# Kernel optimization log

Hardware: AMD Instinct MI355X
Metric: run time of the kernel (lower is better)

## Reference

```python
import jax, jax.numpy as jnp
import numpy as np

N = 2048; K = 2048; D = 256; D_RESHAPE = 800
HA = 256; DA = 128; HK = 128; HC = 128; HS = 256
S = max(10, int(0.1 * K))  # n_sample = 204
BN_SCALE = 1.0 / float(np.sqrt(1.0 + 1e-5))  # eval BatchNorm1d with running stats (0,1)

def leaky(x):
    return jax.nn.leaky_relu(x, 0.01)

def conv2d(x, w, b):
    y = jax.lax.conv_general_dilated(x, w, (1, 1), 'VALID', dimension_numbers=('NCHW', 'OIHW', 'NCHW'))
    return y + b[None, :, None, None]

def maxpool2(x):
    return jax.lax.reduce_window(x, -jnp.inf, jax.lax.max, (1, 1, 2, 2), (1, 1, 2, 2), 'VALID')

def data_transform(x, c1w, c1b, c2w, c2b, ew, eb):
    h = maxpool2(leaky(conv2d(x, c1w, c1b)))   # [n,20,12,12]
    h = maxpool2(leaky(conv2d(h, c2w, c2b)))   # [n,50,4,4]
    h = h.reshape(-1, D_RESHAPE)
    return leaky(h @ ew.T + eb)                # [n,D]

def skip_block(X, w1, b1, w2, b2, w3, b3):
    # Conv1d kernel_size=1 == per-position linear over channels
    X1 = leaky(X @ w1.T + b1) * BN_SCALE       # [n,HC]
    X2 = leaky(X @ w2.T + b2) * BN_SCALE       # [n,HC]
    X3 = leaky(X @ w3.T + b3) * BN_SCALE       # [n,d]
    feat = jax.nn.softmax(X1 @ X2.T, axis=0)   # torch Softmax(dim=1) on [1,n,n] -> axis 0
    return feat @ X3 + X

def mask_scores(A, w1, b1, w2, b2, w3, b3, w4, b4):
    X1 = leaky(A @ w1.T + b1)                  # [n,HK]
    X2 = jnp.tanh(A @ w2.T + b2)               # [n,HK]
    M = X1.T @ X2                              # [HK,HK]
    A3 = leaky(M @ w3.T + b3)                  # [HK,K]
    s = A3.T @ w4[0] + b4[0]                   # [K]
    return jax.nn.softmax(s)

def attention(X, few, feb, vw, vb, uw, ub, aww, awb, ew, eb):
    H = leaky(X @ few.T + feb)                 # [n,HA]
    AV = jnp.tanh(H @ vw.T + vb)
    AU = leaky(H @ uw.T + ub)
    a = leaky((AV * AU) @ aww.T + awb)         # [n,1]
    A = jax.nn.softmax(a.T, axis=1)            # [1,n]
    M = leaky((A @ H) @ ew.T + eb)             # [1,d]
    return M, A

def euclid(X, Y):
    d2 = jnp.sum(X * X, 1)[:, None] + jnp.sum(Y * Y, 1)[None, :] - 2.0 * (X @ Y.T)
    return jnp.sqrt(jnp.maximum(d2, 0.0))


def setup_inputs() -> dict:
    key = jax.random.key(0)
    ks = iter(jax.random.split(key, 70))
    def rn(shape, scale=0.05):
        return jax.random.normal(next(ks), shape, dtype=jnp.float32) * scale
    d = {}
    d['B'] = jax.random.normal(next(ks), (N, 1, 28, 28), dtype=jnp.float32)
    d['KB'] = jax.random.normal(next(ks), (K, 1, 28, 28), dtype=jnp.float32)
    d['dt_c1_w'] = rn((20, 1, 5, 5)); d['dt_c1_b'] = rn((20,))
    d['dt_c2_w'] = rn((50, 20, 5, 5)); d['dt_c2_b'] = rn((50,))
    d['dt_emb_w'] = rn((D, D_RESHAPE)); d['dt_emb_b'] = rn((D,))
    for nm, dd in (('sk1', D), ('sk2', D), ('sk3', K)):
        d[nm + '_w1'] = rn((HC, dd)); d[nm + '_b1'] = rn((HC,))
        d[nm + '_w2'] = rn((HC, dd)); d[nm + '_b2'] = rn((HC,))
        d[nm + '_w3'] = rn((dd, dd)); d[nm + '_b3'] = rn((dd,))
    d['mk_w1'] = rn((HK, K)); d['mk_b1'] = rn((HK,))
    d['mk_w2'] = rn((HK, K)); d['mk_b2'] = rn((HK,))
    d['mk_w3'] = rn((K, HK)); d['mk_b3'] = rn((K,))
    d['mk_w4'] = rn((1, HK)); d['mk_b4'] = rn((1,))
    d['fuse_w'] = rn((D, D + S)); d['fuse_b'] = rn((D,))
    for nm, din in (('a1', D), ('a2', 2 * D)):
        d[nm + '_fe_w'] = rn((HA, din)); d[nm + '_fe_b'] = rn((HA,))
        d[nm + '_v_w'] = rn((DA, HA)); d[nm + '_v_b'] = rn((DA,))
        d[nm + '_u_w'] = rn((DA, HA)); d[nm + '_u_b'] = rn((DA,))
        d[nm + '_aw_w'] = rn((1, DA)); d[nm + '_aw_b'] = rn((1,))
        d[nm + '_emb_w'] = rn((din, HA)); d[nm + '_emb_b'] = rn((din,))
    d['semb_w'] = rn((HS, 2 * D)); d['semb_b'] = rn((HS,))
    d['cls_w'] = rn((1, HS)); d['cls_b'] = rn((1,))
    return d


def reference(B, KB, dt_c1_w, dt_c1_b, dt_c2_w, dt_c2_b, dt_emb_w, dt_emb_b,
              sk1_w1, sk1_b1, sk1_w2, sk1_b2, sk1_w3, sk1_b3,
              sk2_w1, sk2_b1, sk2_w2, sk2_b2, sk2_w3, sk2_b3,
              sk3_w1, sk3_b1, sk3_w2, sk3_b2, sk3_w3, sk3_b3,
              mk_w1, mk_b1, mk_w2, mk_b2, mk_w3, mk_b3, mk_w4, mk_b4,
              fuse_w, fuse_b,
              a1_fe_w, a1_fe_b, a1_v_w, a1_v_b, a1_u_w, a1_u_b, a1_aw_w, a1_aw_b, a1_emb_w, a1_emb_b,
              a2_fe_w, a2_fe_b, a2_v_w, a2_v_b, a2_u_w, a2_u_b, a2_aw_w, a2_aw_b, a2_emb_w, a2_emb_b,
              semb_w, semb_b, cls_w, cls_b):
    B_dt = data_transform(B, dt_c1_w, dt_c1_b, dt_c2_w, dt_c2_b, dt_emb_w, dt_emb_b)
    KB_dt = data_transform(KB, dt_c1_w, dt_c1_b, dt_c2_w, dt_c2_b, dt_emb_w, dt_emb_b)
    Xs = skip_block(B_dt, sk1_w1, sk1_b1, sk1_w2, sk1_b2, sk1_w3, sk1_b3)
    Ks = skip_block(KB_dt, sk2_w1, sk2_b1, sk2_w2, sk2_b2, sk2_w3, sk2_b3)
    # torch detaches the affinity (.detach().numpy())
    aff = euclid(jax.lax.stop_gradient(Xs), jax.lax.stop_gradient(Ks))  # [N,K]
    aff_s = skip_block(aff, sk3_w1, sk3_b1, sk3_w2, sk3_b2, sk3_w3, sk3_b3)
    scores = mask_scores(aff_s, mk_w1, mk_b1, mk_w2, mk_b2, mk_w3, mk_b3, mk_w4, mk_b4)
    idx = jnp.argsort(-scores)[:S]                       # top-S knowledge columns
    B_bag = jax.nn.softmax(aff_s[:, idx], axis=1)        # [N,S], torch Softmax(dim=2)
    B_fuse = leaky(jnp.concatenate([B_dt, B_bag], axis=1) @ fuse_w.T + fuse_b)  # [N,D]
    M1, _ = attention(B_fuse, a1_fe_w, a1_fe_b, a1_v_w, a1_v_b, a1_u_w, a1_u_b, a1_aw_w, a1_aw_b, a1_emb_w, a1_emb_b)
    X2 = jnp.concatenate([B_fuse, jnp.tile(M1, (B_fuse.shape[0], 1))], axis=1)  # [N,2D]
    bvec, A = attention(X2, a2_fe_w, a2_fe_b, a2_v_w, a2_v_b, a2_u_w, a2_u_b, a2_aw_w, a2_aw_b, a2_emb_w, a2_emb_b)
    bvec = leaky(bvec @ semb_w.T + semb_b)               # [1,HS]
    Y = jnp.clip(jax.nn.sigmoid(bvec @ cls_w.T + cls_b), 1e-5, 1.0 - 1e-5)
    return (Y, A)
```

## Files before the change

kernel.cpp:

```cpp
#include <hip/hip_runtime.h>
#include <math.h>

#define LEAKY(x) ((x) > 0.f ? (x) : 0.01f * (x))
static constexpr float BN_SCALE = 0.9999950000374997f;

typedef unsigned short ushort_t;
typedef float f32x4 __attribute__((ext_vector_type(4)));
typedef short bf16x8 __attribute__((ext_vector_type(8)));

__device__ __forceinline__ ushort_t f2bfu(float f) {
  union { float f; unsigned u; } v; v.f = f;
  unsigned r = v.u + 0x7fffu + ((v.u >> 16) & 1u);
  return (ushort_t)(r >> 16);
}
__device__ __forceinline__ float bfu2f(ushort_t u) {
  union { unsigned u; float f; } v; v.u = ((unsigned)u) << 16;
  return v.f;
}

__device__ __forceinline__ void gload16(const ushort_t* g, ushort_t* lds) {
  __builtin_amdgcn_global_load_lds(
      (const __attribute__((address_space(1))) void*)g,
      (__attribute__((address_space(3))) void*)lds, 16, 0, 0);
}

__global__ void fill_out(float* out, int n) {
  int i = blockIdx.x * 256 + threadIdx.x;
  if (i < n) out[i] = 0.25f;
}

struct CvtArgs {
  const float* src[20];
  ushort_t* dst[20];
  int len[20];
};
__global__ void to_bf16_multi(CvtArgs a) {
  for (int s = 0; s < 20; ++s) {
    const float* sp = a.src[s];
    ushort_t* dp = a.dst[s];
    int n = a.len[s];
    for (int i = blockIdx.x * 256 + threadIdx.x; i < n; i += gridDim.x * 256)
      dp[i] = f2bfu(sp[i]);
  }
}

struct BiasPk { const float* a[12]; float* out; };
__global__ void bias_pack(BiasPk p) {
  int b = blockIdx.x, t = threadIdx.x;
  p.out[b * 256 + t] = (t < 128) ? p.a[2 * b][t] : p.a[2 * b + 1][t - 128];
}

__global__ void pad_fuse_bf16(const float* __restrict__ w, ushort_t* __restrict__ wp) {
  int idx = blockIdx.x * 256 + threadIdx.x;
  if (idx >= 256 * 512) return;
  int o = idx >> 9, k = idx & 511;
  wp[idx] = (k < 460) ? f2bfu(w[(size_t)o * 460 + k]) : (ushort_t)0;
}

__launch_bounds__(256)
__global__ void conv12_mfma(const float* __restrict__ imgB, const float* __restrict__ imgK,
                            const float* __restrict__ w1, const float* __restrict__ b1,
                            const ushort_t* __restrict__ w2b, const float* __restrict__ b2,
                            ushort_t* __restrict__ out800) {
  __shared__ __align__(16) char smem[39168];
  ushort_t* sh1u = (ushort_t*)smem;
  float* simg = (float*)(smem + 11520);
  float* sw1  = (float*)(smem + 18688);
  float* b1s  = (float*)(smem + 20928);
  ushort_t* As = (ushort_t*)(smem + 11520);
  ushort_t* Bs = (ushort_t*)(smem + 29952);
  float* Cf = (float*)smem;

  int tid = threadIdx.x;
  int bx = blockIdx.x;
  const float* imgb = (bx < 1024) ? imgB + (size_t)bx * 2 * 784
                                  : imgK + (size_t)(bx - 1024) * 2 * 784;

  for (int i = tid; i < 1568; i += 256) {
    int im = (i >= 784) ? 1 : 0;
    int r = i - im * 784;
    int row = r / 28, col = r - row * 28;
    int sc = (col + (row >> 1)) & 31;
    simg[im * 896 + row * 32 + sc] = imgb[i];
  }
  for (int i = tid; i < 500; i += 256) sw1[i] = w1[i];
  if (tid < 20) b1s[tid] = b1[tid];
  __syncthreads();

  for (int o = tid; o < 1152; o += 256) {
    int im = (o >= 576) ? 1 : 0;
    int rem = o - im * 576;
    int cg = rem / 144;
    int pos = rem - cg * 144;
    int py = pos / 12, px = pos - py * 12;
    int y0 = py * 2, x0 = px * 2;
    float p[6][6];
    #pragma unroll
    for (int yy = 0; yy < 6; ++yy) {
      int rr = y0 + yy;
      int rbase = im * 896 + rr * 32;
      int rot = rr >> 1;
      #pragma unroll
      for (int xx = 0; xx < 6; ++xx)
        p[yy][xx] = simg[rbase + ((x0 + xx + rot) & 31)];
    }
    #pragma unroll
    for (int cc = 0; cc < 5; ++cc) {
      int c = cg * 5 + cc;
      const float* wc = &sw1[c * 25];
      float bb = b1s[c];
      float t0 = bb, t1 = bb, t2 = bb, t3 = bb;
      #pragma unroll
      for (int ky = 0; ky < 5; ++ky)
        #pragma unroll
        for (int kx = 0; kx < 5; ++kx) {
          float wv = wc[ky * 5 + kx];
          t0 += p[ky][kx] * wv;
          t1 += p[ky][kx + 1] * wv;
          t2 += p[ky + 1][kx] * wv;
          t3 += p[ky + 1][kx + 1] * wv;
        }
      float mx = fmaxf(fmaxf(t0, t1), fmaxf(t2, t3));
      sh1u[im * 2880 + c * 144 + pos] = f2bfu(LEAKY(mx));
    }
  }

  int wave = tid >> 6, lane = tid & 63;
  int wm = (wave >> 1) * 64, wn = (wave & 1) * 32;
  int mrow = lane & 15, kq = lane >> 4;
  int kl = tid & 63, rbase = tid >> 6;

  f32x4 acc[4][2];
  #pragma unroll
  for (int i = 0; i < 4; ++i)
    #pragma unroll
    for (int j = 0; j < 2; ++j)
      #pragma unroll
      for (int r = 0; r < 4; ++r) acc[i][j][r] = 0.f;

  for (int k0 = 0; k0 < 512; k0 += 64) {
    __syncthreads();
    int k = k0 + kl;
    bool valid = k < 500;
    int ic = k / 25, tap = k - ic * 25;
    int ky = tap / 5, kx = tap - ky * 5;
    int kof = ic * 144 + ky * 12 + kx;
    ushort_t tA[32];
    #pragma unroll
    for (int i = 0; i < 32; ++i) {
      int r = rbase + 4 * i;
      int im = r >> 6, pos = r & 63, oy = pos >> 3, ox = pos & 7;
      tA[i] = valid ? sh1u[im * 2880 + kof + oy * 12 + ox] : (ushort_t)0;
    }
    ushort_t tB[16];
    #pragma unroll
    for (int i = 0; i < 16; ++i) {
      int oc = rbase + 4 * i;
      tB[i] = (valid && oc < 50) ? w2b[(size_t)oc * 500 + k] : (ushort_t)0;
    }
    #pragma unroll
    for (int i = 0; i < 32; ++i) As[(rbase + 4 * i) * 72 + kl] = tA[i];
    #pragma unroll
    for (int i = 0; i < 16; ++i) Bs[(rbase + 4 * i) * 72 + kl] = tB[i];
    __syncthreads();
    #pragma unroll
    for (int ks = 0; ks < 2; ++ks) {
      bf16x8 af[4], bf[2];
      #pragma unroll
      for (int mt = 0; mt < 4; ++mt)
        af[mt] = *(const bf16x8*)&As[(wm + mt * 16 + mrow) * 72 + ks * 32 + kq * 8];
      #pragma unroll
      for (int nt = 0; nt < 2; ++nt)
        bf[nt] = *(const bf16x8*)&Bs[(wn + nt * 16 + mrow) * 72 + ks * 32 + kq * 8];
      #pragma unroll
      for (int mt = 0; mt < 4; ++mt)
        #pragma unroll
        for (int nt = 0; nt < 2; ++nt)
          acc[mt][nt] = __builtin_amdgcn_mfma_f32_16x16x32_bf16(af[mt], bf[nt], acc[mt][nt], 0, 0, 0);
    }
  }
  __syncthreads();
  #pragma unroll
  for (int mt = 0; mt < 4; ++mt)
    #pragma unroll
    for (int nt = 0; nt < 2; ++nt) {
      int n0 = wn + nt * 16 + (lane & 15);
      #pragma unroll
      for (int r = 0; r < 4; ++r)
        Cf[(wm + mt * 16 + kq * 4 + r) * 68 + n0] = acc[mt][nt][r];
    }
  __syncthreads();
  for (int o = tid; o < 1600; o += 256) {
    int im = o / 800, oi = o - im * 800;
    int oc = oi >> 4, p = oi & 15, py = p >> 2, px = p & 3;
    int r0 = im * 64 + py * 16 + px * 2;
    float bb = b2[oc];
    float t0 = LEAKY(Cf[r0 * 68 + oc] + bb);
    float t1 = LEAKY(Cf[(r0 + 1) * 68 + oc] + bb);
    float t2 = LEAKY(Cf[(r0 + 8) * 68 + oc] + bb);
    float t3 = LEAKY(Cf[(r0 + 9) * 68 + oc] + bb);
    out800[(size_t)(bx * 2 + im) * 800 + oi] = f2bfu(fmaxf(fmaxf(t0, t1), fmaxf(t2, t3)));
  }
}

enum { EPI_NONE = 0, EPI_LEAKY = 1, EPI_LEAKY_BN = 2, EPI_TANH = 3, EPI_EUCLID = 4,
       EPI_LEAKY_BN_ROW = 5, EPI_RES = 6 };

#define LROW 40

template <int EPI>
__launch_bounds__(256)
__global__ void gemm_bf16_nt(const ushort_t* __restrict__ A, const ushort_t* __restrict__ B,
                             const float* __restrict__ bias, float* __restrict__ C32,
                             ushort_t* __restrict__ C16, int M, int N, int Kd,
                             const float* __restrict__ e1, const float* __restrict__ e2) {
  __shared__ __align__(16) ushort_t As[128 * 32];
  __shared__ __align__(16) ushort_t Bs[128 * 32];
  int tid = threadIdx.x;
  int bm = blockIdx.y * 128, bn = blockIdx.x * 128;
  int wave = tid >> 6, lane = tid & 63;
  int wm = (wave >> 1) * 64, wn = (wave & 1) * 64;
  int mrow = lane & 15, kq = lane >> 4;
  int l0 = tid, l1 = tid + 256;
  const ushort_t* ga0 = A + (size_t)(bm + (l0 >> 2)) * Kd + (l0 & 3) * 8;
  const ushort_t* ga1 = A + (size_t)(bm + (l1 >> 2)) * Kd + (l1 & 3) * 8;
  const ushort_t* gb0 = B + (size_t)(bn + (l0 >> 2)) * Kd + (l0 & 3) * 8;
  const ushort_t* gb1 = B + (size_t)(bn + (l1 >> 2)) * Kd + (l1 & 3) * 8;

  f32x4 acc[4][4];
  #pragma unroll
  for (int i = 0; i < 4; ++i)
    #pragma unroll
    for (int j = 0; j < 4; ++j)
      #pragma unroll
      for (int r = 0; r < 4; ++r) acc[i][j][r] = 0.f;

  for (int k0 = 0; k0 < Kd; k0 += 32) {
    __syncthreads();
    gload16(ga0 + k0, &As[l0 * 8]);
    gload16(ga1 + k0, &As[l1 * 8]);
    gload16(gb0 + k0, &Bs[l0 * 8]);
    gload16(gb1 + k0, &Bs[l1 * 8]);
    __syncthreads();
    bf16x8 af[4], bf[4];
    #pragma unroll
    for (int mt = 0; mt < 4; ++mt)
      af[mt] = *(const bf16x8*)&As[(wm + mt * 16 + mrow) * 32 + kq * 8];
    #pragma unroll
    for (int nt = 0; nt < 4; ++nt)
      bf[nt] = *(const bf16x8*)&Bs[(wn + nt * 16 + mrow) * 32 + kq * 8];
    #pragma unroll
    for (int mt = 0; mt < 4; ++mt)
      #pragma unroll
      for (int nt = 0; nt < 4; ++nt)
        acc[mt][nt] = __builtin_amdgcn_mfma_f32_16x16x32_bf16(af[mt], bf[nt], acc[mt][nt], 0, 0, 0);
  }
  #pragma unroll
  for (int mt = 0; mt < 4; ++mt)
    #pragma unroll
    for (int nt = 0; nt < 4; ++nt) {
      int n_g = bn + wn + nt * 16 + (lane & 15);
      #pragma unroll
      for (int r = 0; r < 4; ++r) {
        int m_g = bm + wm + mt * 16 + kq * 4 + r;
        float v = acc[mt][nt][r];
        if (EPI == EPI_EUCLID) {
          v = e1[m_g] + e2[n_g] - 2.f * v;
          v = sqrtf(fmaxf(v, 0.f));
        } else if (EPI == EPI_RES) {
          v += bfu2f(((const ushort_t*)e1)[(size_t)m_g * N + n_g]);
        } else {
          if (bias) v += bias[(EPI == EPI_LEAKY_BN_ROW) ? m_g : n_g];
          if (EPI == EPI_LEAKY) v = LEAKY(v);
          else if (EPI == EPI_LEAKY_BN || EPI == EPI_LEAKY_BN_ROW) { v = LEAKY(v); v *= BN_SCALE; }
          else if (EPI == EPI_TANH) v = tanhf(v);
        }
        if (C32) C32[(size_t)m_g * N + n_g] = v;
        if (C16) C16[(size_t)m_g * N + n_g] = f2bfu(v);
      }
    }
}

__launch_bounds__(256)
__global__ void gemm_smat_z(const ushort_t* __restrict__ X12, ushort_t* __restrict__ Smat) {
  int z = blockIdx.z;
  const ushort_t* A = X12 + (size_t)z * 2048 * 256;
  const ushort_t* B = A + 128;
  ushort_t* C = Smat + (size_t)z * 2048 * 2048;
  __shared__ __align__(16) ushort_t As[128 * 32];
  __shared__ __align__(16) ushort_t Bs[128 * 32];
  int tid = threadIdx.x;
  int bm = blockIdx.y * 128, bn = blockIdx.x * 128;
  int wave = tid >> 6, lane = tid & 63;
  int wm = (wave >> 1) * 64, wn = (wave & 1) * 64;
  int mrow = lane & 15, kq = lane >> 4;
  int l0 = tid, l1 = tid + 256;
  const ushort_t* ga0 = A + (size_t)(bm + (l0 >> 2)) * 256 + (l0 & 3) * 8;
  const ushort_t* ga1 = A + (size_t)(bm + (l1 >> 2)) * 256 + (l1 & 3) * 8;
  const ushort_t* gb0 = B + (size_t)(bn + (l0 >> 2)) * 256 + (l0 & 3) * 8;
  const ushort_t* gb1 = B + (size_t)(bn + (l1 >> 2)) * 256 + (l1 & 3) * 8;

  f32x4 acc[4][4];
  #pragma unroll
  for (int i = 0; i < 4; ++i)
    #pragma unroll
    for (int j = 0; j < 4; ++j)
      #pragma unroll
      for (int r = 0; r < 4; ++r) acc[i][j][r] = 0.f;

  for (int k0 = 0; k0 < 128; k0 += 32) {
    __syncthreads();
    gload16(ga0 + k0, &As[l0 * 8]);
    gload16(ga1 + k0, &As[l1 * 8]);
    gload16(gb0 + k0, &Bs[l0 * 8]);
    gload16(gb1 + k0, &Bs[l1 * 8]);
    __syncthreads();
    bf16x8 af[4], bf[4];
    #pragma unroll
    for (int mt = 0; mt < 4; ++mt)
      af[mt] = *(const bf16x8*)&As[(wm + mt * 16 + mrow) * 32 + kq * 8];
    #pragma unroll
    for (int nt = 0; nt < 4; ++nt)
      bf[nt] = *(const bf16x8*)&Bs[(wn + nt * 16 + mrow) * 32 + kq * 8];
    #pragma unroll
    for (int mt = 0; mt < 4; ++mt)
      #pragma unroll
      for (int nt = 0; nt < 4; ++nt)
        acc[mt][nt] = __builtin_amdgcn_mfma_f32_16x16x32_bf16(af[mt], bf[nt], acc[mt][nt], 0, 0, 0);
  }
  #pragma unroll
  for (int mt = 0; mt < 4; ++mt)
    #pragma unroll
    for (int nt = 0; nt < 4; ++nt) {
      int n_g = bn + wn + nt * 16 + (lane & 15);
      #pragma unroll
      for (int r = 0; r < 4; ++r) {
        int m_g = bm + wm + mt * 16 + kq * 4 + r;
        C[(size_t)m_g * 2048 + n_g] = f2bfu(acc[mt][nt][r]);
      }
    }
}

template <int EPI>
__launch_bounds__(256)
__global__ void gemm_bf16_nt64(const ushort_t* __restrict__ A, const ushort_t* __restrict__ B,
                               const float* __restrict__ bias, float* __restrict__ C32,
                               ushort_t* __restrict__ C16, int M, int N, int Kd) {
  __shared__ __align__(16) ushort_t As[64 * 32];
  __shared__ __align__(16) ushort_t Bs[64 * 32];
  int tid = threadIdx.x;
  int bm = blockIdx.y * 64, bn = blockIdx.x * 64;
  int wave = tid >> 6, lane = tid & 63;
  int wm = (wave >> 1) * 32, wn = (wave & 1) * 32;
  int mrow = lane & 15, kq = lane >> 4;
  const ushort_t* ga = A + (size_t)(bm + (tid >> 2)) * Kd + (tid & 3) * 8;
  const ushort_t* gb = B + (size_t)(bn + (tid >> 2)) * Kd + (tid & 3) * 8;

  f32x4 acc[2][2];
  #pragma unroll
  for (int i = 0; i < 2; ++i)
    #pragma unroll
    for (int j = 0; j < 2; ++j)
      #pragma unroll
      for (int r = 0; r < 4; ++r) acc[i][j][r] = 0.f;

  for (int k0 = 0; k0 < Kd; k0 += 32) {
    __syncthreads();
    gload16(ga + k0, &As[tid * 8]);
    gload16(gb + k0, &Bs[tid * 8]);
    __syncthreads();
    bf16x8 af[2], bf[2];
    #pragma unroll
    for (int mt = 0; mt < 2; ++mt)
      af[mt] = *(const bf16x8*)&As[(wm + mt * 16 + mrow) * 32 + kq * 8];
    #pragma unroll
    for (int nt = 0; nt < 2; ++nt)
      bf[nt] = *(const bf16x8*)&Bs[(wn + nt * 16 + mrow) * 32 + kq * 8];
    #pragma unroll
    for (int mt = 0; mt < 2; ++mt)
      #pragma unroll
      for (int nt = 0; nt < 2; ++nt)
        acc[mt][nt] = __builtin_amdgcn_mfma_f32_16x16x32_bf16(af[mt], bf[nt], acc[mt][nt], 0, 0, 0);
  }
  #pragma unroll
  for (int mt = 0; mt < 2; ++mt)
    #pragma unroll
    for (int nt = 0; nt < 2; ++nt) {
      int n_g = bn + wn + nt * 16 + (lane & 15);
      #pragma unroll
      for (int r = 0; r < 4; ++r) {
        int m_g = bm + wm + mt * 16 + kq * 4 + r;
        float v = acc[mt][nt][r];
        if (bias) v += bias[n_g];
        if (EPI == EPI_LEAKY) v = LEAKY(v);
        else if (EPI == EPI_LEAKY_BN) { v = LEAKY(v); v *= BN_SCALE; }
        else if (EPI == EPI_TANH) v = tanhf(v);
        if (C32) C32[(size_t)m_g * N + n_g] = v;
        if (C16) C16[(size_t)m_g * N + n_g] = f2bfu(v);
      }
    }
}

template <int EPI>
__launch_bounds__(256)
__global__ void gemm_nt64_dual(const ushort_t* __restrict__ A, const ushort_t* __restrict__ B1,
                               const ushort_t* __restrict__ B2, const float* __restrict__ bias1,
                               const float* __restrict__ bias2, ushort_t* __restrict__ C16,
                               int M, int N, int Kd, int Msplit) {
  __shared__ __align__(16) ushort_t As[64 * 32];
  __shared__ __align__(16) ushort_t Bs[64 * 32];
  int tid = threadIdx.x;
  int bm = blockIdx.y * 64, bn = blockIdx.x * 64;
  const ushort_t* B = (bm < Msplit) ? B1 : B2;
  const float* bias = (bm < Msplit) ? bias1 : bias2;
  int wave = tid >> 6, lane = tid & 63;
  int wm = (wave >> 1) * 32, wn = (wave & 1) * 32;
  int mrow = lane & 15, kq = lane >> 4;
  const ushort_t* ga = A + (size_t)(bm + (tid >> 2)) * Kd + (tid & 3) * 8;
  const ushort_t* gb = B + (size_t)(bn + (tid >> 2)) * Kd + (tid & 3) * 8;

  f32x4 acc[2][2];
  #pragma unroll
  for (int i = 0; i < 2; ++i)
    #pragma unroll
    for (int j = 0; j < 2; ++j)
      #pragma unroll
      for (int r = 0; r < 4; ++r) acc[i][j][r] = 0.f;

  for (int k0 = 0; k0 < Kd; k0 += 32) {
    __syncthreads();
    gload16(ga + k0, &As[tid * 8]);
    gload16(gb + k0, &Bs[tid * 8]);
    __syncthreads();
    bf16x8 af[2], bf[2];
    #pragma unroll
    for (int mt = 0; mt < 2; ++mt)
      af[mt] = *(const bf16x8*)&As[(wm + mt * 16 + mrow) * 32 + kq * 8];
    #pragma unroll
    for (int nt = 0; nt < 2; ++nt)
      bf[nt] = *(const bf16x8*)&Bs[(wn + nt * 16 + mrow) * 32 + kq * 8];
    #pragma unroll
    for (int mt = 0; mt < 2; ++mt)
      #pragma unroll
      for (int nt = 0; nt < 2; ++nt)
        acc[mt][nt] = __builtin_amdgcn_mfma_f32_16x16x32_bf16(af[mt], bf[nt], acc[mt][nt], 0, 0, 0);
  }
  #pragma unroll
  for (int mt = 0; mt < 2; ++mt)
    #pragma unroll
    for (int nt = 0; nt < 2; ++nt) {
      int n_g = bn + wn + nt * 16 + (lane & 15);
      #pragma unroll
      for (int r = 0; r < 4; ++r) {
        int m_g = bm + wm + mt * 16 + kq * 4 + r;
        float v = acc[mt][nt][r] + bias[n_g];
        if (EPI == EPI_LEAKY) v = LEAKY(v);
        else if (EPI == EPI_LEAKY_BN) { v = LEAKY(v); v *= BN_SCALE; }
        C16[(size_t)m_g * N + n_g] = f2bfu(v);
      }
    }
}

template <int EPI1, int EPI2>
__launch_bounds__(256)
__global__ void gemm_nt64_split(const ushort_t* __restrict__ A, const ushort_t* __restrict__ B,
                                const float* __restrict__ biasPk, float* __restrict__ C32,
                                ushort_t* __restrict__ C16, int M, int N, int Kd, int Nsplit) {
  __shared__ __align__(16) ushort_t As[64 * 32];
  __shared__ __align__(16) ushort_t Bs[64 * 32];
  int tid = threadIdx.x;
  int bm = blockIdx.y * 64, bn = blockIdx.x * 64;
  int wave = tid >> 6, lane = tid & 63;
  int wm = (wave >> 1) * 32, wn = (wave & 1) * 32;
  int mrow = lane & 15, kq = lane >> 4;
  const ushort_t* ga = A + (size_t)(bm + (tid >> 2)) * Kd + (tid & 3) * 8;
  const ushort_t* gb = B + (size_t)(bn + (tid >> 2)) * Kd + (tid & 3) * 8;

  f32x4 acc[2][2];
  #pragma unroll
  for (int i = 0; i < 2; ++i)
    #pragma unroll
    for (int j = 0; j < 2; ++j)
      #pragma unroll
      for (int r = 0; r < 4; ++r) acc[i][j][r] = 0.f;

  for (int k0 = 0; k0 < Kd; k0 += 32) {
    __syncthreads();
    gload16(ga + k0, &As[tid * 8]);
    gload16(gb + k0, &Bs[tid * 8]);
    __syncthreads();
    bf16x8 af[2], bf[2];
    #pragma unroll
    for (int mt = 0; mt < 2; ++mt)
      af[mt] = *(const bf16x8*)&As[(wm + mt * 16 + mrow) * 32 + kq * 8];
    #pragma unroll
    for (int nt = 0; nt < 2; ++nt)
      bf[nt] = *(const bf16x8*)&Bs[(wn + nt * 16 + mrow) * 32 + kq * 8];
    #pragma unroll
    for (int mt = 0; mt < 2; ++mt)
      #pragma unroll
      for (int nt = 0; nt < 2; ++nt)
        acc[mt][nt] = __builtin_amdgcn_mfma_f32_16x16x32_bf16(af[mt], bf[nt], acc[mt][nt], 0, 0, 0);
  }
  #pragma unroll
  for (int mt = 0; mt < 2; ++mt)
    #pragma unroll
    for (int nt = 0; nt < 2; ++nt) {
      int n_g = bn + wn + nt * 16 + (lane & 15);
      #pragma unroll
      for (int r = 0; r < 4; ++r) {
        int m_g = bm + wm + mt * 16 + kq * 4 + r;
        float v = acc[mt][nt][r] + biasPk[n_g];
        if (n_g < Nsplit) {
          if (EPI1 == EPI_LEAKY) v = LEAKY(v);
          else if (EPI1 == EPI_TANH) v = tanhf(v);
        } else {
          if (EPI2 == EPI_LEAKY) v = LEAKY(v);
          else if (EPI2 == EPI_TANH) v = tanhf(v);
        }
        if (C32) C32[(size_t)m_g * N + n_g] = v;
        if (C16) C16[(size_t)m_g * N + n_g] = f2bfu(v);
      }
    }
}

__launch_bounds__(256)
__global__ void gemm_w3T_z(const ushort_t* __restrict__ W3a, const ushort_t* __restrict__ W3b,
                           const float* __restrict__ b3a, const float* __restrict__ b3b,
                           const ushort_t* __restrict__ dtb, ushort_t* __restrict__ X3T) {
  const int N = 2048, Kd = 256;
  int z = blockIdx.z;
  const ushort_t* A = z ? W3b : W3a;
  const float* bias = z ? b3b : b3a;
  const ushort_t* B = dtb + (size_t)z * 2048 * 256;
  ushort_t* C = X3T + (size_t)z * 256 * 2048;
  __shared__ __align__(16) ushort_t As[64 * 32];
  __shared__ __align__(16) ushort_t Bs[64 * 32];
  int tid = threadIdx.x;
  int bm = blockIdx.y * 64, bn = blockIdx.x * 64;
  int wave = tid >> 6, lane = tid & 63;
  int wm = (wave >> 1) * 32, wn = (wave & 1) * 32;
  int mrow = lane & 15, kq = lane >> 4;
  const ushort_t* ga = A + (size_t)(bm + (tid >> 2)) * Kd + (tid & 3) * 8;
  const ushort_t* gb = B + (size_t)(bn + (tid >> 2)) * Kd + (tid & 3) * 8;

  f32x4 acc[2][2];
  #pragma unroll
  for (int i = 0; i < 2; ++i)
    #pragma unroll
    for (int j = 0; j < 2; ++j)
      #pragma unroll
      for (int r = 0; r < 4; ++r) acc[i][j][r] = 0.f;

  for (int k0 = 0; k0 < Kd; k0 += 32) {
    __syncthreads();
    gload16(ga + k0, &As[tid * 8]);
    gload16(gb + k0, &Bs[tid * 8]);
    __syncthreads();
    bf16x8 af[2], bf[2];
    #pragma unroll
    for (int mt = 0; mt < 2; ++mt)
      af[mt] = *(const bf16x8*)&As[(wm + mt * 16 + mrow) * 32 + kq * 8];
    #pragma unroll
    for (int nt = 0; nt < 2; ++nt)
      bf[nt] = *(const bf16x8*)&Bs[(wn + nt * 16 + mrow) * 32 + kq * 8];
    #pragma unroll
    for (int mt = 0; mt < 2; ++mt)
      #pragma unroll
      for (int nt = 0; nt < 2; ++nt)
        acc[mt][nt] = __builtin_amdgcn_mfma_f32_16x16x32_bf16(af[mt], bf[nt], acc[mt][nt], 0, 0, 0);
  }
  #pragma unroll
  for (int mt = 0; mt < 2; ++mt)
    #pragma unroll
    for (int nt = 0; nt < 2; ++nt) {
      int n_g = bn + wn + nt * 16 + (lane & 15);
      #pragma unroll
      for (int r = 0; r < 4; ++r) {
        int m_g = bm + wm + mt * 16 + kq * 4 + r;
        float v = acc[mt][nt][r] + bias[m_g];
        v = LEAKY(v); v *= BN_SCALE;
        C[(size_t)m_g * N + n_g] = f2bfu(v);
      }
    }
}

__launch_bounds__(256)
__global__ void gemm_ntt_res64_z(const ushort_t* __restrict__ SmatBase,
                                 const ushort_t* __restrict__ X3T,
                                 const ushort_t* __restrict__ dtb,
                                 ushort_t* __restrict__ XsKs) {
  const int N = 256, Kd = 2048;
  int z = blockIdx.z;
  const ushort_t* A = SmatBase + (size_t)z * 2048 * 2048;
  const ushort_t* B = X3T + (size_t)z * 256 * 2048;
  const ushort_t* R = dtb + (size_t)z * 2048 * 256;
  ushort_t* C = XsKs + (size_t)z * 2048 * 256;
  __shared__ __align__(16) ushort_t As[64 * 32];
  __shared__ __align__(16) ushort_t Bs[64 * 32];
  int tid = threadIdx.x;
  int bm = blockIdx.y * 64, bn = blockIdx.x * 64;
  int wave = tid >> 6, lane = tid & 63;
  int wm = (wave >> 1) * 32, wn = (wave & 1) * 32;
  int mrow = lane & 15, kq = lane >> 4;
  const ushort_t* ga = A + (size_t)(bm + (tid >> 2)) * Kd + (tid & 3) * 8;
  const ushort_t* gb = B + (size_t)(bn + (tid >> 2)) * Kd + (tid & 3) * 8;

  f32x4 acc[2][2];
  #pragma unroll
  for (int i = 0; i < 2; ++i)
    #pragma unroll
    for (int j = 0; j < 2; ++j)
      #pragma unroll
      for (int r = 0; r < 4; ++r) acc[i][j][r] = 0.f;

  for (int k0 = 0; k0 < Kd; k0 += 32) {
    __syncthreads();
    gload16(ga + k0, &As[tid * 8]);
    gload16(gb + k0, &Bs[tid * 8]);
    __syncthreads();
    bf16x8 af[2], bf[2];
    #pragma unroll
    for (int mt = 0; mt < 2; ++mt)
      af[mt] = *(const bf16x8*)&As[(wm + mt * 16 + mrow) * 32 + kq * 8];
    #pragma unroll
    for (int nt = 0; nt < 2; ++nt)
      bf[nt] = *(const bf16x8*)&Bs[(wn + nt * 16 + mrow) * 32 + kq * 8];
    #pragma unroll
    for (int mt = 0; mt < 2; ++mt)
      #pragma unroll
      for (int nt = 0; nt < 2; ++nt)
        acc[mt][nt] = __builtin_amdgcn_mfma_f32_16x16x32_bf16(af[mt], bf[nt], acc[mt][nt], 0, 0, 0);
  }
  #pragma unroll
  for (int mt = 0; mt < 2; ++mt)
    #pragma unroll
    for (int nt = 0; nt < 2; ++nt) {
      int n_g = bn + wn + nt * 16 + (lane & 15);
      #pragma unroll
      for (int r = 0; r < 4; ++r) {
        int m_g = bm + wm + mt * 16 + kq * 4 + r;
        float v = acc[mt][nt][r] + bfu2f(R[(size_t)m_g * N + n_g]);
        C[(size_t)m_g * N + n_g] = f2bfu(v);
      }
    }
}

__global__ void gemm_tn_part(const ushort_t* __restrict__ X, float* __restrict__ part) {
  int tx = threadIdx.x & 15, ty = threadIdx.x >> 4;
  int i = blockIdx.y * 16 + ty, j = blockIdx.x * 16 + tx;
  int ks = blockIdx.z;
  float acc = 0.f;
  for (int k = ks * 128; k < ks * 128 + 128; ++k)
    acc += bfu2f(X[(size_t)k * 256 + i]) * bfu2f(X[(size_t)k * 256 + 128 + j]);
  part[(size_t)ks * 16384 + i * 128 + j] = acc;
}
__global__ void gemm_tn_reduce(const float* __restrict__ part, ushort_t* __restrict__ Mm) {
  int idx = blockIdx.x * 256 + threadIdx.x;
  float s = 0.f;
  #pragma unroll
  for (int ks = 0; ks < 16; ++ks) s += part[(size_t)ks * 16384 + idx];
  Mm[idx] = f2bfu(s);
}

__global__ void smax_partA(const ushort_t* __restrict__ Sb, float* __restrict__ pm,
                           float* __restrict__ pl, int N) {
  int z = blockIdx.z;
  const ushort_t* S = Sb + (size_t)z * 2048 * 2048;
  int t = threadIdx.x;
  int col = blockIdx.x * 64 + (t & 63);
  int g = t >> 6;
  int r0 = blockIdx.y * 128 + g;
  float vals[32];
  #pragma unroll
  for (int i = 0; i < 32; ++i)
    vals[i] = bfu2f(S[(size_t)(r0 + 4 * i) * N + col]);
  float m = -1e30f;
  #pragma unroll
  for (int i = 0; i < 32; ++i) m = fmaxf(m, vals[i]);
  float l = 0.f;
  #pragma unroll
  for (int i = 0; i < 32; ++i) l += expf(vals[i] - m);
  __shared__ float rm[4][64], rl[4][64];
  rm[g][t & 63] = m; rl[g][t & 63] = l;
  __syncthreads();
  if (g == 0) {
    int c = t & 63;
    float M0 = rm[0][c], L0 = rl[0][c];
    #pragma unroll
    for (int j = 1; j < 4; ++j) {
      float Mj = rm[j][c], Lj = rl[j][c];
      float nm = fmaxf(M0, Mj);
      L0 = L0 * expf(M0 - nm) + Lj * expf(Mj - nm);
      M0 = nm;
    }
    pm[((size_t)z * 16 + blockIdx.y) * N + col] = M0;
    pl[((size_t)z * 16 + blockIdx.y) * N + col] = L0;
  }
}
__global__ void smax_partB(const float* __restrict__ pm, const float* __restrict__ pl,
                           float* __restrict__ gm, float* __restrict__ gi, int N) {
  int z = blockIdx.y;
  int col = blockIdx.x * 256 + threadIdx.x;
  float m = -1e30f, l = 0.f;
  for (int b = 0; b < 16; ++b) {
    float bm = pm[((size_t)z * 16 + b) * N + col], bl = pl[((size_t)z * 16 + b) * N + col];
    float nm = fmaxf(m, bm);
    l = l * expf(m - nm) + bl * expf(bm - nm);
    m = nm;
  }
  gm[(size_t)z * N + col] = m;
  gi[(size_t)z * N + col] = 1.f / l;
}
__global__ void smax_partC(ushort_t* __restrict__ Sb, const float* __restrict__ gm,
                           const float* __restrict__ gi, int N) {
  int z = blockIdx.z;
  ushort_t* S = Sb + (size_t)z * 2048 * 2048;
  int t = threadIdx.x;
  int col = blockIdx.x * 64 + (t & 63);
  int g = t >> 6;
  float m = gm[(size_t)z * N + col], inv = gi[(size_t)z * N + col];
  int r0 = blockIdx.y * 128 + g;
  #pragma unroll 8
  for (int i = 0; i < 32; ++i) {
    size_t idx = (size_t)(r0 + 4 * i) * N + col;
    S[idx] = f2bfu(expf(bfu2f(S[idx]) - m) * inv);
  }
}

__global__ void row_norm_bf16(const ushort_t* __restrict__ X, float* __restrict__ out, int Kd) {
  int r = blockIdx.x;
  int t = threadIdx.x;
  float s = 0.f;
  for (int k = t; k < Kd; k += 64) { float v = bfu2f(X[(size_t)r * Kd + k]); s += v * v; }
  for (int off = 32; off; off >>= 1) s += __shfl_down(s, off);
  if (t == 0) out[r] = s;
}

__global__ void mask_score(const float* __restrict__ A3, const float* __restrict__ w4,
                           const float* __restrict__ b4, float* __restrict__ s) {
  int k = blockIdx.x * 256 + threadIdx.x;
  float acc = b4[0];
  for (int h = 0; h < 128; ++h) acc += A3[(size_t)h * 2048 + k] * w4[h];
  s[k] = acc;
}

__global__ void topk_rank(const float* __restrict__ s, int* __restrict__ idx, int K, int S) {
  __shared__ float sv[2048];
  int t = threadIdx.x;
  for (int i = t; i < K; i += 256) sv[i] = s[i];
  __syncthreads();
  int j = blockIdx.x * 256 + t;
  if (j >= K) return;
  float sj = sv[j];
  int rank = 0;
  #pragma unroll 8
  for (int i = 0; i < 2048; ++i) {
    float si = sv[i];
    rank += (si > sj) || (si == sj && i < j);
  }
  if (rank < S) idx[rank] = j;
}

__global__ void build_cat(const ushort_t* __restrict__ Bdt, const ushort_t* __restrict__ affs,
                          const int* __restrict__ idx, ushort_t* __restrict__ cat) {
  int r = blockIdx.x, t = threadIdx.x;
  __shared__ float vals[256];
  __shared__ float red[256];
  float v = -1e30f;
  if (t < 204) {
    int ix = idx[t];
    ix = ix < 0 ? 0 : (ix > 2047 ? 2047 : ix);
    v = bfu2f(affs[(size_t)r * 2048 + ix]);
  }
  vals[t] = v;
  red[t] = v;
  __syncthreads();
  for (int off = 128; off; off >>= 1) { if (t < off) red[t] = fmaxf(red[t], red[t + off]); __syncthreads(); }
  float m = red[0];
  __syncthreads();
  float e = (t < 204) ? expf(vals[t] - m) : 0.f;
  red[t] = e;
  __syncthreads();
  for (int off = 128; off; off >>= 1) { if (t < off) red[t] += red[t + off]; __syncthreads(); }
  float inv = 1.f / red[0];
  cat[(size_t)r * 512 + t] = Bdt[(size_t)r * 256 + t];
  cat[(size_t)r * 512 + 256 + t] = (t < 204) ? f2bfu(e * inv) : (ushort_t)0;
}

__global__ void attn_gate(const float* __restrict__ AVU, const float* __restrict__ aww,
                          const float* __restrict__ awb, float* __restrict__ a, int n) {
  int wave = threadIdx.x >> 6, lane = threadIdx.x & 63;
  int r = blockIdx.x * 4 + wave;
  if (r >= n) return;
  float s = 0.f;
  #pragma unroll
  for (int j = 0; j < 2; ++j) {
    int d = lane + 64 * j;
    s += AVU[(size_t)r * 256 + d] * AVU[(size_t)r * 256 + 128 + d] * aww[d];
  }
  for (int off = 32; off; off >>= 1) s += __shfl_down(s, off);
  if (lane == 0) {
    float acc = s + awb[0];
    a[r] = LEAKY(acc);
  }
}

__global__ void softmax_vec(const float* __restrict__ x, float* __restrict__ y,
                            float* __restrict__ y2, int n) {
  __shared__ float red[256];
  int t = threadIdx.x;
  float m = -1e30f;
  for (int i = t; i < n; i += 256) m = fmaxf(m, x[i]);
  red[t] = m;
  __syncthreads();
  for (int off = 128; off; off >>= 1) { if (t < off) red[t] = fmaxf(red[t], red[t + off]); __syncthreads(); }
  m = red[0];
  __syncthreads();
  float s = 0.f;
  for (int i = t; i < n; i += 256) s += expf(x[i] - m);
  red[t] = s;
  __syncthreads();
  for (int off = 128; off; off >>= 1) { if (t < off) red[t] += red[t + off]; __syncthreads(); }
  float inv = 1.f / red[0];
  for (int i = t; i < n; i += 256) {
    float v = expf(x[i] - m) * inv;
    y[i] = v;
    if (y2) y2[i] = v;
  }
}

__global__ void colsum_part(const float* __restrict__ wv, const ushort_t* __restrict__ H,
                            float* __restrict__ part, int n) {
  int bk = blockIdx.x, c = threadIdx.x;
  float s = 0.f;
  for (int r = bk; r < n; r += 16) s += wv[r] * bfu2f(H[(size_t)r * 256 + c]);
  part[bk * 256 + c] = s;
}
__global__ void colsum_fin(const float* __restrict__ part, float* __restrict__ out) {
  int c = threadIdx.x;
  float s = 0.f;
  #pragma unroll
  for (int k = 0; k < 16; ++k) s += part[k * 256 + c];
  out[c] = s;
}

__global__ void gemv_act(const float* __restrict__ x, const float* __restrict__ W,
                         const float* __restrict__ b, float* __restrict__ out,
                         int O, int Kd, int act) {
  int o = blockIdx.x * blockDim.x + threadIdx.x;
  if (o >= O) return;
  float acc = b ? b[o] : 0.f;
  for (int k = 0; k < Kd; ++k) acc += x[k] * W[(size_t)o * Kd + k];
  if (act == 1) acc = LEAKY(acc);
  out[o] = acc;
}

__global__ void build_cat2(const ushort_t* __restrict__ Bf, const float* __restrict__ M1,
                           ushort_t* __restrict__ cat2) {
  int r = blockIdx.x, t = threadIdx.x;
  cat2[(size_t)r * 512 + t] = (t < 256) ? Bf[(size_t)r * 256 + t] : f2bfu(M1[t - 256]);
}

__global__ void final_head(const float* __restrict__ AH2, const float* __restrict__ embw,
                           const float* __restrict__ embb, const float* __restrict__ sembw,
                           const float* __restrict__ sembb, const float* __restrict__ clsw,
                           const float* __restrict__ clsb, float* __restrict__ Yout) {
  __shared__ float bvec[512];
  __shared__ float red[512];
  int t = threadIdx.x;
  float acc = embb[t];
  for (int c = 0; c < 256; ++c) acc += AH2[c] * embw[(size_t)t * 256 + c];
  bvec[t] = LEAKY(acc);
  __syncthreads();
  float p = 0.f;
  if (t < 256) {
    float a2 = sembb[t];
    for (int c = 0; c < 512; ++c) a2 += bvec[c] * sembw[(size_t)t * 512 + c];
    a2 = LEAKY(a2);
    p = a2 * clsw[t];
  }
  red[t] = p;
  __syncthreads();
  for (int off = 256; off; off >>= 1) { if (t < off) red[t] += red[t + off]; __syncthreads(); }
  if (t == 0) {
    float y = red[0] + clsb[0];
    y = 1.f / (1.f + expf(-y));
    y = fminf(fmaxf(y, 1e-5f), 1.f - 1e-5f);
    Yout[0] = y;
  }
}

extern "C" void kernel_launch(void* const* d_in, const int* in_sizes, int n_in,
                              void* d_out, int out_size, void* d_ws, size_t ws_size,
                              hipStream_t stream) {
  auto IN = [&](int i) { return (const float*)d_in[i]; };
  (void)n_in; (void)in_sizes; (void)out_size;

  const int S = 204;
  float* out_f = (float*)d_out;

  float* W = (float*)d_ws;
  size_t off = 0;
  auto F = [&](size_t n) { float* p = W + off; off += n; return p; };
  auto FU = [&](size_t nus) { return (ushort_t*)F((nus + 1) / 2); };

  ushort_t* dt_b  = FU((size_t)4096 * 256);
  ushort_t* XsKs  = FU((size_t)4096 * 256);
  ushort_t* X12b  = FU((size_t)4096 * 256);
  ushort_t* X3sb  = FU((size_t)4096 * 256);
  ushort_t* aff_b = FU((size_t)2048 * 2048);
  float* AVU   = F((size_t)2048 * 256);
  ushort_t* Mm_b = FU((size_t)128 * 128);
  float* svec  = F(2048);
  int*   idxb  = (int*)F(256);
  float* avec  = F(2048);
  float* Awv   = F(2048);
  float* AH    = F(256);
  float* M1v   = F(256);
  float* AH2   = F(256);
  float* nxy   = F(4096);
  float* part  = F(4096);
  float* sm_pm = F((size_t)2 * 16 * 2048);
  float* sm_pl = F((size_t)2 * 16 * 2048);
  float* sm_gm = F(2 * 2048);
  float* sm_gi = F(2 * 2048);
  float* pbias = F(6 * 256);

  size_t wo = 0;
  ushort_t* warena = (ushort_t*)F(3227872);
  auto WA = [&](size_t n) { ushort_t* p = warena + wo; wo = (wo + n + 15) & ~(size_t)15; return p; };
  ushort_t* w2b   = WA(25000);
  ushort_t* embb_ = WA(204800);
  ushort_t* s1w1 = WA(32768); ushort_t* s1w2 = WA(32768); ushort_t* s1w3 = WA(65536);
  ushort_t* s2w1 = WA(32768); ushort_t* s2w2 = WA(32768); ushort_t* s2w3 = WA(65536);
  ushort_t* s3w1 = WA(262144); ushort_t* s3w2 = WA(262144); ushort_t* s3w3 = WA(4194304);
  ushort_t* mw1 = WA(262144); ushort_t* mw2 = WA(262144); ushort_t* mw3 = WA(262144);
  ushort_t* fwp = WA(131072);
  ushort_t* a1fe = WA(65536); ushort_t* a1v = WA(32768); ushort_t* a1u = WA(32768);
  ushort_t* a2fe = WA(131072); ushort_t* a2v = WA(32768); ushort_t* a2u = WA(32768);
  (void)s1w2; (void)s2w2; (void)s3w2; (void)mw2; (void)a1u; (void)a2u;

  float* pool = F((size_t)4194304);

  const size_t NEED_BYTES = off * 4;
  if (ws_size < NEED_BYTES) {
    fill_out<<<9, 256, 0, stream>>>(out_f, 2049);
    return;
  }

  ushort_t* h2h_b   = (ushort_t*)pool;
  ushort_t* SmatB   = (ushort_t*)pool;
  ushort_t* X3b_b   = (ushort_t*)(pool + 2097152);
  float* A3   = pool;
  float* tnpt = pool + 262144;
  ushort_t* cat_b   = (ushort_t*)pool;
  ushort_t* cat2_b  = (ushort_t*)(pool + 524288);
  ushort_t* Bfuse_b = (ushort_t*)(pool + 1048576);
  ushort_t* Hbuf_b  = (ushort_t*)(pool + 1310720);

  CvtArgs ca;
  const float* srcs[20] = { IN(4), IN(6), IN(8), IN(10), IN(12), IN(14), IN(16), IN(18),
                            IN(20), IN(22), IN(24), IN(26), IN(28), IN(30),
                            IN(36), IN(38), IN(40), IN(46), IN(48), IN(50) };
  ushort_t* dsts[20] = { w2b, embb_, s1w1, s1w2, s1w3, s2w1, s2w2, s2w3,
                         s3w1, s3w2, s3w3, mw1, mw2, mw3,
                         a1fe, a1v, a1u, a2fe, a2v, a2u };
  int lens[20] = { 25000, 204800, 32768, 32768, 65536, 32768, 32768, 65536,
                   262144, 262144, 4194304, 262144, 262144, 262144,
                   65536, 32768, 32768, 131072, 32768, 32768 };
  for (int i = 0; i < 20; ++i) { ca.src[i] = srcs[i]; ca.dst[i] = dsts[i]; ca.len[i] = lens[i]; }
  to_bf16_multi<<<1024, 256, 0, stream>>>(ca);
  pad_fuse_bf16<<<512, 256, 0, stream>>>(IN(34), fwp);
  BiasPk bp;
  const float* bsrc[12] = { IN(9), IN(11), IN(15), IN(17), IN(21), IN(23),
                            IN(27), IN(29), IN(39), IN(41), IN(49), IN(51) };
  for (int i = 0; i < 12; ++i) bp.a[i] = bsrc[i];
  bp.out = pbias;
  bias_pack<<<6, 256, 0, stream>>>(bp);
  float* pb_sk1 = pbias, *pb_sk2 = pbias + 256, *pb_sk3 = pbias + 512;
  float* pb_msk = pbias + 768, *pb_a1 = pbias + 1024, *pb_a2 = pbias + 1280;

  conv12_mfma<<<2048, 256, 0, stream>>>(IN(0), IN(1), IN(2), IN(3), w2b, IN(5), h2h_b);
  gemm_bf16_nt64<EPI_LEAKY><<<dim3(4, 64), 256, 0, stream>>>(
      h2h_b, embb_, IN(7), nullptr, dt_b, 4096, 256, 800);

  gemm_nt64_dual<EPI_LEAKY_BN><<<dim3(4, 64), 256, 0, stream>>>(
      dt_b, s1w1, s2w1, pb_sk1, pb_sk2, X12b, 4096, 256, 256, 2048);
  gemm_w3T_z<<<dim3(32, 4, 2), 256, 0, stream>>>(s1w3, s2w3, IN(13), IN(19), dt_b, X3sb);
  gemm_smat_z<<<dim3(16, 16, 2), 256, 0, stream>>>(X12b, SmatB);
  smax_partA<<<dim3(32, 16, 2), 256, 0, stream>>>(SmatB, sm_pm, sm_pl, 2048);
  smax_partB<<<dim3(8, 2), 256, 0, stream>>>(sm_pm, sm_pl, sm_gm, sm_gi, 2048);
  smax_partC<<<dim3(32, 16, 2), 256, 0, stream>>>(SmatB, sm_gm, sm_gi, 2048);
  gemm_ntt_res64_z<<<dim3(4, 32, 2), 256, 0, stream>>>(SmatB, X3sb, dt_b, XsKs);

  row_norm_bf16<<<4096, 64, 0, stream>>>(XsKs, nxy, 256);
  gemm_bf16_nt<EPI_EUCLID><<<dim3(16, 16), 256, 0, stream>>>(
      XsKs, XsKs + (size_t)2048 * 256, nullptr, nullptr, aff_b, 2048, 2048, 256,
      nxy, nxy + 2048);

  gemm_bf16_nt64<EPI_LEAKY_BN><<<dim3(4, 32), 256, 0, stream>>>(
      aff_b, s3w1, pb_sk3, nullptr, X12b, 2048, 256, 2048);
  gemm_smat_z<<<dim3(16, 16, 1), 256, 0, stream>>>(X12b, SmatB);
  gemm_bf16_nt<EPI_LEAKY_BN_ROW><<<dim3(16, 16), 256, 0, stream>>>(
      s3w3, aff_b, IN(25), nullptr, X3b_b, 2048, 2048, 2048, nullptr, nullptr);
  smax_partA<<<dim3(32, 16, 1), 256, 0, stream>>>(SmatB, sm_pm, sm_pl, 2048);
  smax_partB<<<dim3(8, 1), 256, 0, stream>>>(sm_pm, sm_pl, sm_gm, sm_gi, 2048);
  smax_partC<<<dim3(32, 16, 1), 256, 0, stream>>>(SmatB, sm_gm, sm_gi, 2048);
  gemm_bf16_nt<EPI_RES><<<dim3(16, 16), 256, 0, stream>>>(
      SmatB, X3b_b, nullptr, nullptr, aff_b, 2048, 2048, 2048,
      (const float*)aff_b, nullptr);
  ushort_t* affs_b = aff_b;

  gemm_nt64_split<EPI_LEAKY, EPI_TANH><<<dim3(4, 32), 256, 0, stream>>>(
      affs_b, mw1, pb_msk, nullptr, X12b, 2048, 256, 2048, 128);
  gemm_tn_part<<<dim3(8, 8, 16), 256, 0, stream>>>(X12b, tnpt);
  gemm_tn_reduce<<<64, 256, 0, stream>>>(tnpt, Mm_b);
  gemm_bf16_nt64<EPI_LEAKY><<<dim3(32, 2), 256, 0, stream>>>(
      Mm_b, mw3, IN(31), A3, nullptr, 128, 2048, 128);
  mask_score<<<8, 256, 0, stream>>>(A3, IN(32), IN(33), svec);
  topk_rank<<<8, 256, 0, stream>>>(svec, idxb, 2048, S);

  build_cat<<<2048, 256, 0, stream>>>(dt_b, affs_b, idxb, cat_b);
  gemm_bf16_nt64<EPI_LEAKY><<<dim3(4, 32), 256, 0, stream>>>(
      cat_b, fwp, IN(35), nullptr, Bfuse_b, 2048, 256, 512);

  gemm_bf16_nt64<EPI_LEAKY><<<dim3(4, 32), 256, 0, stream>>>(
      Bfuse_b, a1fe, IN(37), nullptr, Hbuf_b, 2048, 256, 256);
  gemm_nt64_split<EPI_TANH, EPI_LEAKY><<<dim3(4, 32), 256, 0, stream>>>(
      Hbuf_b, a1v, pb_a1, AVU, nullptr, 2048, 256, 256, 128);
  attn_gate<<<512, 256, 0, stream>>>(AVU, IN(42), IN(43), avec, 2048);
  softmax_vec<<<1, 256, 0, stream>>>(avec, Awv, nullptr, 2048);
  colsum_part<<<16, 256, 0, stream>>>(Awv, Hbuf_b, part, 2048);
  colsum_fin<<<1, 256, 0, stream>>>(part, AH);
  gemv_act<<<1, 256, 0, stream>>>(AH, IN(44), IN(45), M1v, 256, 256, 1);
  build_cat2<<<2048, 512, 0, stream>>>(Bfuse_b, M1v, cat2_b);

  gemm_bf16_nt64<EPI_LEAKY><<<dim3(4, 32), 256, 0, stream>>>(
      cat2_b, a2fe, IN(47), nullptr, Hbuf_b, 2048, 256, 512);
  gemm_nt64_split<EPI_TANH, EPI_LEAKY><<<dim3(4, 32), 256, 0, stream>>>(
      Hbuf_b, a2v, pb_a2, AVU, nullptr, 2048, 256, 256, 128);
  attn_gate<<<512, 256, 0, stream>>>(AVU, IN(52), IN(53), avec, 2048);
  softmax_vec<<<1, 256, 0, stream>>>(avec, Awv, out_f + 1, 2048);
  colsum_part<<<16, 256, 0, stream>>>(Awv, Hbuf_b, part, 2048);
  colsum_fin<<<1, 256, 0, stream>>>(part, AH2);

  final_head<<<1, 512, 0, stream>>>(AH2, IN(54), IN(55), IN(56), IN(57),
                                    IN(58), IN(59), out_f);
}
```

Measured before the change: 911.3 us.

## Double-buffer GEMM LDS tiles, relayout conv2 im2col, flatten bf16 conversion

```diff
diff --git a/kernel.cpp b/kernel.cpp
--- a/kernel.cpp
+++ b/kernel.cpp
@@ -32,15 +32,15 @@
 struct CvtArgs {
   const float* src[20];
   ushort_t* dst[20];
-  int len[20];
+  int cum[21];
 };
-__global__ void to_bf16_multi(CvtArgs a) {
-  for (int s = 0; s < 20; ++s) {
-    const float* sp = a.src[s];
-    ushort_t* dp = a.dst[s];
-    int n = a.len[s];
-    for (int i = blockIdx.x * 256 + threadIdx.x; i < n; i += gridDim.x * 256)
-      dp[i] = f2bfu(sp[i]);
+__global__ void to_bf16_flat(CvtArgs a) {
+  int total = a.cum[20];
+  for (int i = blockIdx.x * 256 + threadIdx.x; i < total; i += gridDim.x * 256) {
+    int s = 0;
+    while (i >= a.cum[s + 1]) ++s;
+    int off = i - a.cum[s];
+    a.dst[s][off] = f2bfu(a.src[s][off]);
   }
 }
 
@@ -57,19 +57,30 @@
   wp[idx] = (k < 460) ? f2bfu(w[(size_t)o * 460 + k]) : (ushort_t)0;
 }
 
+__global__ void w2_relayout(const float* __restrict__ w2, ushort_t* __restrict__ w2p) {
+  int idx = blockIdx.x * 256 + threadIdx.x;
+  if (idx >= 64 * 640) return;
+  int oc = idx / 640, k = idx - oc * 640;
+  int tap = k / 24, ic = k - tap * 24;
+  float v = 0.f;
+  if (oc < 50 && tap < 25 && ic < 20)
+    v = w2[(size_t)(oc * 20 + ic) * 25 + tap];
+  w2p[idx] = f2bfu(v);
+}
+
 __launch_bounds__(256)
 __global__ void conv12_mfma(const float* __restrict__ imgB, const float* __restrict__ imgK,
                             const float* __restrict__ w1, const float* __restrict__ b1,
-                            const ushort_t* __restrict__ w2b, const float* __restrict__ b2,
+                            const ushort_t* __restrict__ w2p, const float* __restrict__ b2,
                             ushort_t* __restrict__ out800) {
-  __shared__ __align__(16) char smem[39168];
-  ushort_t* sh1u = (ushort_t*)smem;
-  float* simg = (float*)(smem + 11520);
-  float* sw1  = (float*)(smem + 18688);
-  float* b1s  = (float*)(smem + 20928);
-  ushort_t* As = (ushort_t*)(smem + 11520);
-  ushort_t* Bs = (ushort_t*)(smem + 29952);
-  float* Cf = (float*)smem;
+  __shared__ __align__(16) char smem[41472];
+  ushort_t* h1T = (ushort_t*)smem;
+  ushort_t* As  = (ushort_t*)(smem + 13824);
+  ushort_t* Bs  = (ushort_t*)(smem + 32256);
+  float* simg = (float*)(smem + 13824);
+  float* sw1  = (float*)(smem + 20992);
+  float* b1s  = (float*)(smem + 23040);
+  float* Cf   = (float*)smem;
 
   int tid = threadIdx.x;
   int bx = blockIdx.x;
@@ -85,6 +96,10 @@
   }
   for (int i = tid; i < 500; i += 256) sw1[i] = w1[i];
   if (tid < 20) b1s[tid] = b1[tid];
+  for (int i = tid; i < 288; i += 256) {
+    uint2 z; z.x = 0; z.y = 0;
+    *(uint2*)&h1T[i * 24 + 20] = z;
+  }
   __syncthreads();
 
   for (int o = tid; o < 1152; o += 256) {
@@ -121,14 +136,21 @@
           t3 += p[ky + 1][kx + 1] * wv;
         }
       float mx = fmaxf(fmaxf(t0, t1), fmaxf(t2, t3));
-      sh1u[im * 2880 + c * 144 + pos] = f2bfu(LEAKY(mx));
+      h1T[(im * 144 + pos) * 24 + c] = f2bfu(LEAKY(mx));
     }
   }
 
   int wave = tid >> 6, lane = tid & 63;
   int wm = (wave >> 1) * 64, wn = (wave & 1) * 32;
   int mrow = lane & 15, kq = lane >> 4;
-  int kl = tid & 63, rbase = tid >> 6;
+
+  int sA_r = tid >> 1;
+  int sA_j0 = (tid & 1) * 4;
+  int sA_im = sA_r >> 6;
+  int sA_op = sA_r & 63;
+  int sA_oy = sA_op >> 3, sA_ox = sA_op & 7;
+  int sB_r = tid >> 2;
+  int sB_j0 = (tid & 3) * 2;
 
   f32x4 acc[4][2];
   #pragma unroll
@@ -138,30 +160,35 @@
       #pragma unroll
       for (int r = 0; r < 4; ++r) acc[i][j][r] = 0.f;
 
-  for (int k0 = 0; k0 < 512; k0 += 64) {
+  bf16x8 wreg[2];
+  #pragma unroll
+  for (int i = 0; i < 2; ++i)
+    wreg[i] = *(const bf16x8*)&w2p[(size_t)sB_r * 640 + (sB_j0 + i) * 8];
+
+  for (int kb = 0; kb < 10; ++kb) {
     __syncthreads();
-    int k = k0 + kl;
-    bool valid = k < 500;
-    int ic = k / 25, tap = k - ic * 25;
-    int ky = tap / 5, kx = tap - ky * 5;
-    int kof = ic * 144 + ky * 12 + kx;
-    ushort_t tA[32];
-    #pragma unroll
-    for (int i = 0; i < 32; ++i) {
-      int r = rbase + 4 * i;
-      int im = r >> 6, pos = r & 63, oy = pos >> 3, ox = pos & 7;
-      tA[i] = valid ? sh1u[im * 2880 + kof + oy * 12 + ox] : (ushort_t)0;
-    }
-    ushort_t tB[16];
-    #pragma unroll
-    for (int i = 0; i < 16; ++i) {
-      int oc = rbase + 4 * i;
-      tB[i] = (valid && oc < 50) ? w2b[(size_t)oc * 500 + k] : (ushort_t)0;
-    }
-    #pragma unroll
-    for (int i = 0; i < 32; ++i) As[(rbase + 4 * i) * 72 + kl] = tA[i];
-    #pragma unroll
-    for (int i = 0; i < 16; ++i) Bs[(rbase + 4 * i) * 72 + kl] = tB[i];
+    #pragma unroll
+    for (int i = 0; i < 2; ++i)
+      *(bf16x8*)&Bs[sB_r * 72 + (sB_j0 + i) * 8] = wreg[i];
+    #pragma unroll
+    for (int i = 0; i < 4; ++i) {
+      int j = sA_j0 + i;
+      int g = kb * 8 + j;
+      int tap = g / 3;
+      int part = g - tap * 3;
+      bf16x8 v = {0, 0, 0, 0, 0, 0, 0, 0};
+      if (tap < 25) {
+        int ky = tap / 5, kx = tap - ky * 5;
+        int pos = (sA_oy + ky) * 12 + sA_ox + kx;
+        v = *(const bf16x8*)&h1T[(sA_im * 144 + pos) * 24 + part * 8];
+      }
+      *(bf16x8*)&As[sA_r * 72 + j * 8] = v;
+    }
+    if (kb + 1 < 10) {
+      #pragma unroll
+      for (int i = 0; i < 2; ++i)
+        wreg[i] = *(const bf16x8*)&w2p[(size_t)sB_r * 640 + (kb + 1) * 64 + (sB_j0 + i) * 8];
+    }
     __syncthreads();
     #pragma unroll
     for (int ks = 0; ks < 2; ++ks) {
@@ -206,16 +233,14 @@
 enum { EPI_NONE = 0, EPI_LEAKY = 1, EPI_LEAKY_BN = 2, EPI_TANH = 3, EPI_EUCLID = 4,
        EPI_LEAKY_BN_ROW = 5, EPI_RES = 6 };
 
-#define LROW 40
-
 template <int EPI>
 __launch_bounds__(256)
 __global__ void gemm_bf16_nt(const ushort_t* __restrict__ A, const ushort_t* __restrict__ B,
                              const float* __restrict__ bias, float* __restrict__ C32,
                              ushort_t* __restrict__ C16, int M, int N, int Kd,
                              const float* __restrict__ e1, const float* __restrict__ e2) {
-  __shared__ __align__(16) ushort_t As[128 * 32];
-  __shared__ __align__(16) ushort_t Bs[128 * 32];
+  __shared__ __align__(16) ushort_t As[2][128 * 32];
+  __shared__ __align__(16) ushort_t Bs[2][128 * 32];
   int tid = threadIdx.x;
   int bm = blockIdx.y * 128, bn = blockIdx.x * 128;
   int wave = tid >> 6, lane = tid & 63;
@@ -235,35 +260,43 @@
       #pragma unroll
       for (int r = 0; r < 4; ++r) acc[i][j][r] = 0.f;
 
-  for (int k0 = 0; k0 < Kd; k0 += 32) {
+  gload16(ga0, &As[0][l0 * 8]);
+  gload16(ga1, &As[0][l1 * 8]);
+  gload16(gb0, &Bs[0][l0 * 8]);
+  gload16(gb1, &Bs[0][l1 * 8]);
+  int nt = Kd >> 5;
+  for (int t = 0; t < nt; ++t) {
+    int cur = t & 1;
     __syncthreads();
-    gload16(ga0 + k0, &As[l0 * 8]);
-    gload16(ga1 + k0, &As[l1 * 8]);
-    gload16(gb0 + k0, &Bs[l0 * 8]);
-    gload16(gb1 + k0, &Bs[l1 * 8]);
-    __syncthreads();
+    if (t + 1 < nt) {
+      int ko = (t + 1) * 32;
+      gload16(ga0 + ko, &As[cur ^ 1][l0 * 8]);
+      gload16(ga1 + ko, &As[cur ^ 1][l1 * 8]);
+      gload16(gb0 + ko, &Bs[cur ^ 1][l0 * 8]);
+      gload16(gb1 + ko, &Bs[cur ^ 1][l1 * 8]);
+    }
     bf16x8 af[4], bf[4];
     #pragma unroll
     for (int mt = 0; mt < 4; ++mt)
-      af[mt] = *(const bf16x8*)&As[(wm + mt * 16 + mrow) * 32 + kq * 8];
-    #pragma unroll
-    for (int nt = 0; nt < 4; ++nt)
-      bf[nt] = *(const bf16x8*)&Bs[(wn + nt * 16 + mrow) * 32 + kq * 8];
+      af[mt] = *(const bf16x8*)&As[cur][(wm + mt * 16 + mrow) * 32 + kq * 8];
+    #pragma unroll
+    for (int nt2 = 0; nt2 < 4; ++nt2)
+      bf[nt2] = *(const bf16x8*)&Bs[cur][(wn + nt2 * 16 + mrow) * 32 + kq * 8];
     #pragma unroll
     for (int mt = 0; mt < 4; ++mt)
       #pragma unroll
-      for (int nt = 0; nt < 4; ++nt)
-        acc[mt][nt] = __builtin_amdgcn_mfma_f32_16x16x32_bf16(af[mt], bf[nt], acc[mt][nt], 0, 0, 0);
+      for (int nt2 = 0; nt2 < 4; ++nt2)
+        acc[mt][nt2] = __builtin_amdgcn_mfma_f32_16x16x32_bf16(af[mt], bf[nt2], acc[mt][nt2], 0, 0, 0);
   }
   #pragma unroll
   for (int mt = 0; mt < 4; ++mt)
     #pragma unroll
-    for (int nt = 0; nt < 4; ++nt) {
-      int n_g = bn + wn + nt * 16 + (lane & 15);
+    for (int nt2 = 0; nt2 < 4; ++nt2) {
+      int n_g = bn + wn + nt2 * 16 + (lane & 15);
       #pragma unroll
       for (int r = 0; r < 4; ++r) {
         int m_g = bm + wm + mt * 16 + kq * 4 + r;
-        float v = acc[mt][nt][r];
+        float v = acc[mt][nt2][r];
         if (EPI == EPI_EUCLID) {
           v = e1[m_g] + e2[n_g] - 2.f * v;
           v = sqrtf(fmaxf(v, 0.f));
@@ -287,8 +320,8 @@
   const ushort_t* A = X12 + (size_t)z * 2048 * 256;
   const ushort_t* B = A + 128;
   ushort_t* C = Smat + (size_t)z * 2048 * 2048;
-  __shared__ __align__(16) ushort_t As[128 * 32];
-  __shared__ __align__(16) ushort_t Bs[128 * 32];
+  __shared__ __align__(16) ushort_t As[2][128 * 32];
+  __shared__ __align__(16) ushort_t Bs[2][128 * 32];
   int tid = threadIdx.x;
   int bm = blockIdx.y * 128, bn = blockIdx.x * 128;
   int wave = tid >> 6, lane = tid & 63;
@@ -308,35 +341,42 @@
       #pragma unroll
       for (int r = 0; r < 4; ++r) acc[i][j][r] = 0.f;
 
-  for (int k0 = 0; k0 < 128; k0 += 32) {
+  gload16(ga0, &As[0][l0 * 8]);
+  gload16(ga1, &As[0][l1 * 8]);
+  gload16(gb0, &Bs[0][l0 * 8]);
+  gload16(gb1, &Bs[0][l1 * 8]);
+  for (int t = 0; t < 4; ++t) {
+    int cur = t & 1;
     __syncthreads();
-    gload16(ga0 + k0, &As[l0 * 8]);
-    gload16(ga1 + k0, &As[l1 * 8]);
-    gload16(gb0 + k0, &Bs[l0 * 8]);
-    gload16(gb1 + k0, &Bs[l1 * 8]);
-    __syncthreads();
+    if (t + 1 < 4) {
+      int ko = (t + 1) * 32;
+      gload16(ga0 + ko, &As[cur ^ 1][l0 * 8]);
+      gload16(ga1 + ko, &As[cur ^ 1][l1 * 8]);
+      gload16(gb0 + ko, &Bs[cur ^ 1][l0 * 8]);
+      gload16(gb1 + ko, &Bs[cur ^ 1][l1 * 8]);
+    }
     bf16x8 af[4], bf[4];
     #pragma unroll
     for (int mt = 0; mt < 4; ++mt)
-      af[mt] = *(const bf16x8*)&As[(wm + mt * 16 + mrow) * 32 + kq * 8];
-    #pragma unroll
-    for (int nt = 0; nt < 4; ++nt)
-      bf[nt] = *(const bf16x8*)&Bs[(wn + nt * 16 + mrow) * 32 + kq * 8];
+      af[mt] = *(const bf16x8*)&As[cur][(wm + mt * 16 + mrow) * 32 + kq * 8];
+    #pragma unroll
+    for (int nt2 = 0; nt2 < 4; ++nt2)
+      bf[nt2] = *(const bf16x8*)&Bs[cur][(wn + nt2 * 16 + mrow) * 32 + kq * 8];
     #pragma unroll
     for (int mt = 0; mt < 4; ++mt)
       #pragma unroll
-      for (int nt = 0; nt < 4; ++nt)
-        acc[mt][nt] = __builtin_amdgcn_mfma_f32_16x16x32_bf16(af[mt], bf[nt], acc[mt][nt], 0, 0, 0);
+      for (int nt2 = 0; nt2 < 4; ++nt2)
+        acc[mt][nt2] = __builtin_amdgcn_mfma_f32_16x16x32_bf16(af[mt], bf[nt2], acc[mt][nt2], 0, 0, 0);
   }
   #pragma unroll
   for (int mt = 0; mt < 4; ++mt)
     #pragma unroll
-    for (int nt = 0; nt < 4; ++nt) {
-      int n_g = bn + wn + nt * 16 + (lane & 15);
+    for (int nt2 = 0; nt2 < 4; ++nt2) {
+      int n_g = bn + wn + nt2 * 16 + (lane & 15);
       #pragma unroll
       for (int r = 0; r < 4; ++r) {
         int m_g = bm + wm + mt * 16 + kq * 4 + r;
-        C[(size_t)m_g * 2048 + n_g] = f2bfu(acc[mt][nt][r]);
+        C[(size_t)m_g * 2048 + n_g] = f2bfu(acc[mt][nt2][r]);
       }
     }
 }
@@ -346,8 +386,8 @@
 __global__ void gemm_bf16_nt64(const ushort_t* __restrict__ A, const ushort_t* __restrict__ B,
                                const float* __restrict__ bias, float* __restrict__ C32,
                                ushort_t* __restrict__ C16, int M, int N, int Kd) {
-  __shared__ __align__(16) ushort_t As[64 * 32];
-  __shared__ __align__(16) ushort_t Bs[64 * 32];
+  __shared__ __align__(16) ushort_t As[2][64 * 32];
+  __shared__ __align__(16) ushort_t Bs[2][64 * 32];
   int tid = threadIdx.x;
   int bm = blockIdx.y * 64, bn = blockIdx.x * 64;
   int wave = tid >> 6, lane = tid & 63;
@@ -364,33 +404,39 @@
       #pragma unroll
       for (int r = 0; r < 4; ++r) acc[i][j][r] = 0.f;
 
-  for (int k0 = 0; k0 < Kd; k0 += 32) {
+  gload16(ga, &As[0][tid * 8]);
+  gload16(gb, &Bs[0][tid * 8]);
+  int nt = Kd >> 5;
+  for (int t = 0; t < nt; ++t) {
+    int cur = t & 1;
     __syncthreads();
-    gload16(ga + k0, &As[tid * 8]);
-    gload16(gb + k0, &Bs[tid * 8]);
-    __syncthreads();
+    if (t + 1 < nt) {
+      int ko = (t + 1) * 32;
+      gload16(ga + ko, &As[cur ^ 1][tid * 8]);
+      gload16(gb + ko, &Bs[cur ^ 1][tid * 8]);
+    }
     bf16x8 af[2], bf[2];
     #pragma unroll
     for (int mt = 0; mt < 2; ++mt)
-      af[mt] = *(const bf16x8*)&As[(wm + mt * 16 + mrow) * 32 + kq * 8];
-    #pragma unroll
-    for (int nt = 0; nt < 2; ++nt)
-      bf[nt] = *(const bf16x8*)&Bs[(wn + nt * 16 + mrow) * 32 + kq * 8];
+      af[mt] = *(const bf16x8*)&As[cur][(wm + mt * 16 + mrow) * 32 + kq * 8];
+    #pragma unroll
+    for (int nt2 = 0; nt2 < 2; ++nt2)
+      bf[nt2] = *(const bf16x8*)&Bs[cur][(wn + nt2 * 16 + mrow) * 32 + kq * 8];
     #pragma unroll
     for (int mt = 0; mt < 2; ++mt)
       #pragma unroll
-      for (int nt = 0; nt < 2; ++nt)
-        acc[mt][nt] = __builtin_amdgcn_mfma_f32_16x16x32_bf16(af[mt], bf[nt], acc[mt][nt], 0, 0, 0);
+      for (int nt2 = 0; nt2 < 2; ++nt2)
+        acc[mt][nt2] = __builtin_amdgcn_mfma_f32_16x16x32_bf16(af[mt], bf[nt2], acc[mt][nt2], 0, 0, 0);
   }
   #pragma unroll
   for (int mt = 0; mt < 2; ++mt)
     #pragma unroll
-    for (int nt = 0; nt < 2; ++nt) {
-      int n_g = bn + wn + nt * 16 + (lane & 15);
+    for (int nt2 = 0; nt2 < 2; ++nt2) {
+      int n_g = bn + wn + nt2 * 16 + (lane & 15);
       #pragma unroll
       for (int r = 0; r < 4; ++r) {
         int m_g = bm + wm + mt * 16 + kq * 4 + r;
-        float v = acc[mt][nt][r];
+        float v = acc[mt][nt2][r];
         if (bias) v += bias[n_g];
         if (EPI == EPI_LEAKY) v = LEAKY(v);
         else if (EPI == EPI_LEAKY_BN) { v = LEAKY(v); v *= BN_SCALE; }
@@ -407,8 +453,8 @@
                                const ushort_t* __restrict__ B2, const float* __restrict__ bias1,
                                const float* __restrict__ bias2, ushort_t* __restrict__ C16,
                                int M, int N, int Kd, int Msplit) {
-  __shared__ __align__(16) ushort_t As[64 * 32];
-  __shared__ __align__(16) ushort_t Bs[64 * 32];
+  __shared__ __align__(16) ushort_t As[2][64 * 32];
+  __shared__ __align__(16) ushort_t Bs[2][64 * 32];
   int tid = threadIdx.x;
   int bm = blockIdx.y * 64, bn = blockIdx.x * 64;
   const ushort_t* B = (bm < Msplit) ? B1 : B2;
@@ -427,33 +473,39 @@
       #pragma unroll
       for (int r = 0; r < 4; ++r) acc[i][j][r] = 0.f;
 
-  for (int k0 = 0; k0 < Kd; k0 += 32) {
+  gload16(ga, &As[0][tid * 8]);
+  gload16(gb, &Bs[0][tid * 8]);
+  int nt = Kd >> 5;
+  for (int t = 0; t < nt; ++t) {
+    int cur = t & 1;
     __syncthreads();
-    gload16(ga + k0, &As[tid * 8]);
-    gload16(gb + k0, &Bs[tid * 8]);
-    __syncthreads();
+    if (t + 1 < nt) {
+      int ko = (t + 1) * 32;
+      gload16(ga + ko, &As[cur ^ 1][tid * 8]);
+      gload16(gb + ko, &Bs[cur ^ 1][tid * 8]);
+    }
     bf16x8 af[2], bf[2];
     #pragma unroll
     for (int mt = 0; mt < 2; ++mt)
-      af[mt] = *(const bf16x8*)&As[(wm + mt * 16 + mrow) * 32 + kq * 8];
-    #pragma unroll
-    for (int nt = 0; nt < 2; ++nt)
-      bf[nt] = *(const bf16x8*)&Bs[(wn + nt * 16 + mrow) * 32 + kq * 8];
+      af[mt] = *(const bf16x8*)&As[cur][(wm + mt * 16 + mrow) * 32 + kq * 8];
+    #pragma unroll
+    for (int nt2 = 0; nt2 < 2; ++nt2)
+      bf[nt2] = *(const bf16x8*)&Bs[cur][(wn + nt2 * 16 + mrow) * 32 + kq * 8];
     #pragma unroll
     for (int mt = 0; mt < 2; ++mt)
       #pragma unroll
-      for (int nt = 0; nt < 2; ++nt)
-        acc[mt][nt] = __builtin_amdgcn_mfma_f32_16x16x32_bf16(af[mt], bf[nt], acc[mt][nt], 0, 0, 0);
+      for (int nt2 = 0; nt2 < 2; ++nt2)
+        acc[mt][nt2] = __builtin_amdgcn_mfma_f32_16x16x32_bf16(af[mt], bf[nt2], acc[mt][nt2], 0, 0, 0);
   }
   #pragma unroll
   for (int mt = 0; mt < 2; ++mt)
     #pragma unroll
-    for (int nt = 0; nt < 2; ++nt) {
-      int n_g = bn + wn + nt * 16 + (lane & 15);
+    for (int nt2 = 0; nt2 < 2; ++nt2) {
+      int n_g = bn + wn + nt2 * 16 + (lane & 15);
       #pragma unroll
       for (int r = 0; r < 4; ++r) {
         int m_g = bm + wm + mt * 16 + kq * 4 + r;
-        float v = acc[mt][nt][r] + bias[n_g];
+        float v = acc[mt][nt2][r] + bias[n_g];
         if (EPI == EPI_LEAKY) v = LEAKY(v);
         else if (EPI == EPI_LEAKY_BN) { v = LEAKY(v); v *= BN_SCALE; }
         C16[(size_t)m_g * N + n_g] = f2bfu(v);
@@ -466,8 +518,8 @@
 __global__ void gemm_nt64_split(const ushort_t* __restrict__ A, const ushort_t* __restrict__ B,
                                 const float* __restrict__ biasPk, float* __restrict__ C32,
                                 ushort_t* __restrict__ C16, int M, int N, int Kd, int Nsplit) {
-  __shared__ __align__(16) ushort_t As[64 * 32];
-  __shared__ __align__(16) ushort_t Bs[64 * 32];
+  __shared__ __align__(16) ushort_t As[2][64 * 32];
+  __shared__ __align__(16) ushort_t Bs[2][64 * 32];
   int tid = threadIdx.x;
   int bm = blockIdx.y * 64, bn = blockIdx.x * 64;
   int wave = tid >> 6, lane = tid & 63;
@@ -484,33 +536,39 @@
       #pragma unroll
       for (int r = 0; r < 4; ++r) acc[i][j][r] = 0.f;
 
-  for (int k0 = 0; k0 < Kd; k0 += 32) {
+  gload16(ga, &As[0][tid * 8]);
+  gload16(gb, &Bs[0][tid * 8]);
+  int nt = Kd >> 5;
+  for (int t = 0; t < nt; ++t) {
+    int cur = t & 1;
     __syncthreads();
-    gload16(ga + k0, &As[tid * 8]);
-    gload16(gb + k0, &Bs[tid * 8]);
-    __syncthreads();
+    if (t + 1 < nt) {
+      int ko = (t + 1) * 32;
+      gload16(ga + ko, &As[cur ^ 1][tid * 8]);
+      gload16(gb + ko, &Bs[cur ^ 1][tid * 8]);
+    }
     bf16x8 af[2], bf[2];
     #pragma unroll
     for (int mt = 0; mt < 2; ++mt)
-      af[mt] = *(const bf16x8*)&As[(wm + mt * 16 + mrow) * 32 + kq * 8];
-    #pragma unroll
-    for (int nt = 0; nt < 2; ++nt)
-      bf[nt] = *(const bf16x8*)&Bs[(wn + nt * 16 + mrow) * 32 + kq * 8];
+      af[mt] = *(const bf16x8*)&As[cur][(wm + mt * 16 + mrow) * 32 + kq * 8];
+    #pragma unroll
+    for (int nt2 = 0; nt2 < 2; ++nt2)
+      bf[nt2] = *(const bf16x8*)&Bs[cur][(wn + nt2 * 16 + mrow) * 32 + kq * 8];
     #pragma unroll
     for (int mt = 0; mt < 2; ++mt)
       #pragma unroll
-      for (int nt = 0; nt < 2; ++nt)
-        acc[mt][nt] = __builtin_amdgcn_mfma_f32_16x16x32_bf16(af[mt], bf[nt], acc[mt][nt], 0, 0, 0);
+      for (int nt2 = 0; nt2 < 2; ++nt2)
+        acc[mt][nt2] = __builtin_amdgcn_mfma_f32_16x16x32_bf16(af[mt], bf[nt2], acc[mt][nt2], 0, 0, 0);
   }
   #pragma unroll
   for (int mt = 0; mt < 2; ++mt)
     #pragma unroll
-    for (int nt = 0; nt < 2; ++nt) {
-      int n_g = bn + wn + nt * 16 + (lane & 15);
+    for (int nt2 = 0; nt2 < 2; ++nt2) {
+      int n_g = bn + wn + nt2 * 16 + (lane & 15);
       #pragma unroll
       for (int r = 0; r < 4; ++r) {
         int m_g = bm + wm + mt * 16 + kq * 4 + r;
-        float v = acc[mt][nt][r] + biasPk[n_g];
+        float v = acc[mt][nt2][r] + biasPk[n_g];
         if (n_g < Nsplit) {
           if (EPI1 == EPI_LEAKY) v = LEAKY(v);
           else if (EPI1 == EPI_TANH) v = tanhf(v);
@@ -534,8 +592,8 @@
   const float* bias = z ? b3b : b3a;
   const ushort_t* B = dtb + (size_t)z * 2048 * 256;
   ushort_t* C = X3T + (size_t)z * 256 * 2048;
-  __shared__ __align__(16) ushort_t As[64 * 32];
-  __shared__ __align__(16) ushort_t Bs[64 * 32];
+  __shared__ __align__(16) ushort_t As[2][64 * 32];
+  __shared__ __align__(16) ushort_t Bs[2][64 * 32];
   int tid = threadIdx.x;
   int bm = blockIdx.y * 64, bn = blockIdx.x * 64;
   int wave = tid >> 6, lane = tid & 63;
@@ -552,33 +610,38 @@
       #pragma unroll
       for (int r = 0; r < 4; ++r) acc[i][j][r] = 0.f;
 
-  for (int k0 = 0; k0 < Kd; k0 += 32) {
+  gload16(ga, &As[0][tid * 8]);
+  gload16(gb, &Bs[0][tid * 8]);
+  for (int t = 0; t < 8; ++t) {
+    int cur = t & 1;
     __syncthreads();
-    gload16(ga + k0, &As[tid * 8]);
-    gload16(gb + k0, &Bs[tid * 8]);
-    __syncthreads();
+    if (t + 1 < 8) {
+      int ko = (t + 1) * 32;
+      gload16(ga + ko, &As[cur ^ 1][tid * 8]);
+      gload16(gb + ko, &Bs[cur ^ 1][tid * 8]);
+    }
     bf16x8 af[2], bf[2];
     #pragma unroll
     for (int mt = 0; mt < 2; ++mt)
-      af[mt] = *(const bf16x8*)&As[(wm + mt * 16 + mrow) * 32 + kq * 8];
-    #pragma unroll
-    for (int nt = 0; nt < 2; ++nt)
-      bf[nt] = *(const bf16x8*)&Bs[(wn + nt * 16 + mrow) * 32 + kq * 8];
+      af[mt] = *(const bf16x8*)&As[cur][(wm + mt * 16 + mrow) * 32 + kq * 8];
+    #pragma unroll
+    for (int nt2 = 0; nt2 < 2; ++nt2)
+      bf[nt2] = *(const bf16x8*)&Bs[cur][(wn + nt2 * 16 + mrow) * 32 + kq * 8];
     #pragma unroll
     for (int mt = 0; mt < 2; ++mt)
       #pragma unroll
-      for (int nt = 0; nt < 2; ++nt)
-        acc[mt][nt] = __builtin_amdgcn_mfma_f32_16x16x32_bf16(af[mt], bf[nt], acc[mt][nt], 0, 0, 0);
+      for (int nt2 = 0; nt2 < 2; ++nt2)
+        acc[mt][nt2] = __builtin_amdgcn_mfma_f32_16x16x32_bf16(af[mt], bf[nt2], acc[mt][nt2], 0, 0, 0);
   }
   #pragma unroll
   for (int mt = 0; mt < 2; ++mt)
     #pragma unroll
-    for (int nt = 0; nt < 2; ++nt) {
-      int n_g = bn + wn + nt * 16 + (lane & 15);
+    for (int nt2 = 0; nt2 < 2; ++nt2) {
+      int n_g = bn + wn + nt2 * 16 + (lane & 15);
       #pragma unroll
       for (int r = 0; r < 4; ++r) {
         int m_g = bm + wm + mt * 16 + kq * 4 + r;
-        float v = acc[mt][nt][r] + bias[m_g];
+        float v = acc[mt][nt2][r] + bias[m_g];
         v = LEAKY(v); v *= BN_SCALE;
         C[(size_t)m_g * N + n_g] = f2bfu(v);
       }
@@ -596,8 +659,8 @@
   const ushort_t* B = X3T + (size_t)z * 256 * 2048;
   const ushort_t* R = dtb + (size_t)z * 2048 * 256;
   ushort_t* C = XsKs + (size_t)z * 2048 * 256;
-  __shared__ __align__(16) ushort_t As[64 * 32];
-  __shared__ __align__(16) ushort_t Bs[64 * 32];
+  __shared__ __align__(16) ushort_t As[2][64 * 32];
+  __shared__ __align__(16) ushort_t Bs[2][64 * 32];
   int tid = threadIdx.x;
   int bm = blockIdx.y * 64, bn = blockIdx.x * 64;
   int wave = tid >> 6, lane = tid & 63;
@@ -614,33 +677,38 @@
       #pragma unroll
       for (int r = 0; r < 4; ++r) acc[i][j][r] = 0.f;
 
-  for (int k0 = 0; k0 < Kd; k0 += 32) {
+  gload16(ga, &As[0][tid * 8]);
+  gload16(gb, &Bs[0][tid * 8]);
+  for (int t = 0; t < 64; ++t) {
+    int cur = t & 1;
     __syncthreads();
-    gload16(ga + k0, &As[tid * 8]);
-    gload16(gb + k0, &Bs[tid * 8]);
-    __syncthreads();
+    if (t + 1 < 64) {
+      int ko = (t + 1) * 32;
+      gload16(ga + ko, &As[cur ^ 1][tid * 8]);
+      gload16(gb + ko, &Bs[cur ^ 1][tid * 8]);
+    }
     bf16x8 af[2], bf[2];
     #pragma unroll
     for (int mt = 0; mt < 2; ++mt)
-      af[mt] = *(const bf16x8*)&As[(wm + mt * 16 + mrow) * 32 + kq * 8];
-    #pragma unroll
-    for (int nt = 0; nt < 2; ++nt)
-      bf[nt] = *(const bf16x8*)&Bs[(wn + nt * 16 + mrow) * 32 + kq * 8];
+      af[mt] = *(const bf16x8*)&As[cur][(wm + mt * 16 + mrow) * 32 + kq * 8];
+    #pragma unroll
+    for (int nt2 = 0; nt2 < 2; ++nt2)
+      bf[nt2] = *(const bf16x8*)&Bs[cur][(wn + nt2 * 16 + mrow) * 32 + kq * 8];
     #pragma unroll
     for (int mt = 0; mt < 2; ++mt)
       #pragma unroll
-      for (int nt = 0; nt < 2; ++nt)
-        acc[mt][nt] = __builtin_amdgcn_mfma_f32_16x16x32_bf16(af[mt], bf[nt], acc[mt][nt], 0, 0, 0);
+      for (int nt2 = 0; nt2 < 2; ++nt2)
+        acc[mt][nt2] = __builtin_amdgcn_mfma_f32_16x16x32_bf16(af[mt], bf[nt2], acc[mt][nt2], 0, 0, 0);
   }
   #pragma unroll
   for (int mt = 0; mt < 2; ++mt)
     #pragma unroll
-    for (int nt = 0; nt < 2; ++nt) {
-      int n_g = bn + wn + nt * 16 + (lane & 15);
+    for (int nt2 = 0; nt2 < 2; ++nt2) {
+      int n_g = bn + wn + nt2 * 16 + (lane & 15);
       #pragma unroll
       for (int r = 0; r < 4; ++r) {
         int m_g = bm + wm + mt * 16 + kq * 4 + r;
-        float v = acc[mt][nt][r] + bfu2f(R[(size_t)m_g * N + n_g]);
+        float v = acc[mt][nt2][r] + bfu2f(R[(size_t)m_g * N + n_g]);
         C[(size_t)m_g * N + n_g] = f2bfu(v);
       }
     }
@@ -729,12 +797,14 @@
 }
 
 __global__ void row_norm_bf16(const ushort_t* __restrict__ X, float* __restrict__ out, int Kd) {
-  int r = blockIdx.x;
-  int t = threadIdx.x;
+  int r = blockIdx.x * 2 + (threadIdx.x >> 5);
+  int l = threadIdx.x & 31;
+  bf16x8 v = *(const bf16x8*)&X[(size_t)r * Kd + l * 8];
   float s = 0.f;
-  for (int k = t; k < Kd; k += 64) { float v = bfu2f(X[(size_t)r * Kd + k]); s += v * v; }
-  for (int off = 32; off; off >>= 1) s += __shfl_down(s, off);
-  if (t == 0) out[r] = s;
+  #pragma unroll
+  for (int j = 0; j < 8; ++j) { float f = bfu2f((ushort_t)v[j]); s += f * f; }
+  for (int off = 16; off; off >>= 1) s += __shfl_down(s, off, 32);
+  if (l == 0) out[r] = s;
 }
 
 __global__ void mask_score(const float* __restrict__ A3, const float* __restrict__ w4,
@@ -928,9 +998,9 @@
   float* pbias = F(6 * 256);
 
   size_t wo = 0;
-  ushort_t* warena = (ushort_t*)F(3227872);
+  ushort_t* warena = (ushort_t*)F(3250000);
   auto WA = [&](size_t n) { ushort_t* p = warena + wo; wo = (wo + n + 15) & ~(size_t)15; return p; };
-  ushort_t* w2b   = WA(25000);
+  ushort_t* w2p   = WA(40960);
   ushort_t* embb_ = WA(204800);
   ushort_t* s1w1 = WA(32768); ushort_t* s1w2 = WA(32768); ushort_t* s1w3 = WA(65536);
   ushort_t* s2w1 = WA(32768); ushort_t* s2w2 = WA(32768); ushort_t* s2w3 = WA(65536);
@@ -960,17 +1030,23 @@
   ushort_t* Hbuf_b  = (ushort_t*)(pool + 1310720);
 
   CvtArgs ca;
-  const float* srcs[20] = { IN(4), IN(6), IN(8), IN(10), IN(12), IN(14), IN(16), IN(18),
+  const float* srcs[20] = { IN(6), IN(8), IN(10), IN(12), IN(14), IN(16), IN(18),
                             IN(20), IN(22), IN(24), IN(26), IN(28), IN(30),
-                            IN(36), IN(38), IN(40), IN(46), IN(48), IN(50) };
-  ushort_t* dsts[20] = { w2b, embb_, s1w1, s1w2, s1w3, s2w1, s2w2, s2w3,
+                            IN(36), IN(38), IN(40), IN(46), IN(48), IN(50), IN(4) };
+  ushort_t* dsts[20] = { embb_, s1w1, s1w2, s1w3, s2w1, s2w2, s2w3,
                          s3w1, s3w2, s3w3, mw1, mw2, mw3,
-                         a1fe, a1v, a1u, a2fe, a2v, a2u };
-  int lens[20] = { 25000, 204800, 32768, 32768, 65536, 32768, 32768, 65536,
+                         a1fe, a1v, a1u, a2fe, a2v, a2u, w2p };
+  int lens[20] = { 204800, 32768, 32768, 65536, 32768, 32768, 65536,
                    262144, 262144, 4194304, 262144, 262144, 262144,
-                   65536, 32768, 32768, 131072, 32768, 32768 };
-  for (int i = 0; i < 20; ++i) { ca.src[i] = srcs[i]; ca.dst[i] = dsts[i]; ca.len[i] = lens[i]; }
-  to_bf16_multi<<<1024, 256, 0, stream>>>(ca);
+                   65536, 32768, 32768, 131072, 32768, 32768, 0 };
+  int cum = 0;
+  for (int i = 0; i < 20; ++i) {
+    ca.src[i] = srcs[i]; ca.dst[i] = dsts[i];
+    ca.cum[i] = cum; cum += lens[i];
+  }
+  ca.cum[20] = cum;
+  to_bf16_flat<<<2048, 256, 0, stream>>>(ca);
+  w2_relayout<<<160, 256, 0, stream>>>(IN(4), w2p);
   pad_fuse_bf16<<<512, 256, 0, stream>>>(IN(34), fwp);
   BiasPk bp;
   const float* bsrc[12] = { IN(9), IN(11), IN(15), IN(17), IN(21), IN(23),
@@ -981,7 +1057,7 @@
   float* pb_sk1 = pbias, *pb_sk2 = pbias + 256, *pb_sk3 = pbias + 512;
   float* pb_msk = pbias + 768, *pb_a1 = pbias + 1024, *pb_a2 = pbias + 1280;
 
-  conv12_mfma<<<2048, 256, 0, stream>>>(IN(0), IN(1), IN(2), IN(3), w2b, IN(5), h2h_b);
+  conv12_mfma<<<2048, 256, 0, stream>>>(IN(0), IN(1), IN(2), IN(3), w2p, IN(5), h2h_b);
   gemm_bf16_nt64<EPI_LEAKY><<<dim3(4, 64), 256, 0, stream>>>(
       h2h_b, embb_, IN(7), nullptr, dt_b, 4096, 256, 800);
 
@@ -994,7 +1070,7 @@
   smax_partC<<<dim3(32, 16, 2), 256, 0, stream>>>(SmatB, sm_gm, sm_gi, 2048);
   gemm_ntt_res64_z<<<dim3(4, 32, 2), 256, 0, stream>>>(SmatB, X3sb, dt_b, XsKs);
 
-  row_norm_bf16<<<4096, 64, 0, stream>>>(XsKs, nxy, 256);
+  row_norm_bf16<<<2048, 64, 0, stream>>>(XsKs, nxy, 256);
   gemm_bf16_nt<EPI_EUCLID><<<dim3(16, 16), 256, 0, stream>>>(
       XsKs, XsKs + (size_t)2048 * 256, nullptr, nullptr, aff_b, 2048, 2048, 256,
       nxy, nxy + 2048);
```

Measured after the change: 908.9 us. Within noise of the previous version (-0.3%).
